# Optimization experiments

Measured on AMD Instinct MI355X. Metric: run time of the kernel, lower is better.

Reference implementation:

```python
import jax, jax.numpy as jnp
from jax import lax
import numpy as np

MS = 128            # local_map_size
HALF = MS // 2
B, S = 8, 64
C, H, W = 3, 1024, 1024


def setup_inputs() -> dict:
    key = jax.random.key(0)
    ks = jax.random.split(key, 48)
    r = lambda i, shape, s: jax.random.normal(ks[i], shape, jnp.float32) * s
    z = lambda *shape: jnp.zeros(shape, jnp.float32)
    o = lambda *shape: jnp.ones(shape, jnp.float32)
    return {
        "full_map": jax.random.normal(ks[0], (B, C, H, W), jnp.float32),
        "conditions": jax.random.uniform(ks[1], (B, 5), jnp.float32, 0.0, 1024.0),
        "input_seq": jax.random.uniform(ks[2], (B, S, 2), jnp.float32, 0.0, 1024.0),
        "steps_remaining": jax.random.uniform(ks[3], (B, S), jnp.float32, 0.0, 500.0),
        # LocalMapEncoder convs (OIHW) + batchnorm affine params
        "cw1": r(4, (16, 3, 3, 3), 0.2),   "cb1": z(16),  "g1": o(16),  "be1": z(16),
        "cw2": r(5, (32, 16, 3, 3), 0.1),  "cb2": z(32),  "g2": o(32),  "be2": z(32),
        "cw3": r(6, (64, 32, 3, 3), 0.07), "cb3": z(64),  "g3": o(64),  "be3": z(64),
        "cw4": r(7, (128, 64, 3, 3), 0.05),"cb4": z(128), "g4": o(128), "be4": z(128),
        "fw1": r(8, (512, 128 * 8 * 8), 0.01), "fb1": z(512),
        "fw2": r(9, (256, 512), 0.04),         "fb2": z(256),
        # ConditionEncoder (6 -> 128 -> 64)
        "ew1": r(10, (128, 6), 0.05),  "eb1": z(128),
        "ew2": r(11, (64, 128), 0.05), "eb2": z(64),
        # coord embedder (2 -> 32)
        "mw": r(12, (32, 2), 0.05), "mb": z(32),
        # 2-layer LSTM, torch gate order (i, f, g, o)
        "w_ih0": r(13, (4 * 256, 32), 0.05),  "w_hh0": r(14, (4 * 256, 256), 0.05),
        "b_ih0": z(4 * 256), "b_hh0": z(4 * 256),
        "w_ih1": r(15, (4 * 256, 256), 0.05), "w_hh1": r(16, (4 * 256, 256), 0.05),
        "b_ih1": z(4 * 256), "b_hh1": z(4 * 256),
        # context layer (256+256+64=576 -> 128 -> 64) and output (64 -> 2)
        "xw1": r(17, (128, 576), 0.04), "xb1": z(128),
        "xw2": r(18, (64, 128), 0.05),  "xb2": z(64),
        "ow": r(19, (2, 64), 0.1),      "ob": z(2),
    }


def _conv_bn_relu(x, w, b, g, be):
    # stride-2 3x3 conv, padding 1, NCHW/OIHW; BatchNorm in training mode (batch stats)
    y = lax.conv_general_dilated(x, w, (2, 2), ((1, 1), (1, 1)),
                                 dimension_numbers=("NCHW", "OIHW", "NCHW"))
    y = y + b[None, :, None, None]
    mu = y.mean((0, 2, 3), keepdims=True)
    var = y.var((0, 2, 3), keepdims=True)
    y = (y - mu) * lax.rsqrt(var + 1e-5) * g[None, :, None, None] + be[None, :, None, None]
    return jax.nn.relu(y)


def _lstm_layer(x, w_ih, w_hh, b_ih, b_hh):
    # x: [B, S, D] -> hidden states [B, S, Hd]
    bsz, hd = x.shape[0], w_hh.shape[1]
    bias = b_ih + b_hh
    def step(carry, xt):
        h, c = carry
        zg = xt @ w_ih.T + h @ w_hh.T + bias
        i, f, gg, oo = jnp.split(zg, 4, axis=-1)
        c = jax.nn.sigmoid(f) * c + jax.nn.sigmoid(i) * jnp.tanh(gg)
        h = jax.nn.sigmoid(oo) * jnp.tanh(c)
        return (h, c), h
    h0 = jnp.zeros((bsz, hd), x.dtype)
    _, hs = lax.scan(step, (h0, h0), x.transpose(1, 0, 2))
    return hs.transpose(1, 0, 2)


def reference(full_map, conditions, input_seq, steps_remaining,
              cw1, cb1, g1, be1, cw2, cb2, g2, be2,
              cw3, cb3, g3, be3, cw4, cb4, g4, be4,
              fw1, fb1, fw2, fb2, ew1, eb1, ew2, eb2, mw, mb,
              w_ih0, w_hh0, b_ih0, b_hh0, w_ih1, w_hh1, b_ih1, b_hh1,
              xw1, xb1, xw2, xb2, ow, ob):
    bsz, seq, _ = input_seq.shape
    # --- batched crop+pad gather (replaces host numpy loop): zero-pad map by
    # HALF on each side, then every crop is a dynamic_slice of size MS at (y, x).
    padded = jnp.pad(full_map, ((0, 0), (0, 0), (HALF, HALF), (HALF, HALF)))
    ys = input_seq[..., 0].astype(jnp.int32).reshape(-1)
    xs = input_seq[..., 1].astype(jnp.int32).reshape(-1)
    bidx = jnp.repeat(jnp.arange(bsz, dtype=jnp.int32), seq)
    crop_one = lambda b, y, x: lax.dynamic_slice(padded, (b, 0, y, x), (1, C, MS, MS))[0]
    crops = jax.vmap(crop_one)(bidx, ys, xs)              # [B*S, C, MS, MS]
    # --- LocalMapEncoder
    h = _conv_bn_relu(crops, cw1, cb1, g1, be1)
    h = _conv_bn_relu(h, cw2, cb2, g2, be2)
    h = _conv_bn_relu(h, cw3, cb3, g3, be3)
    h = _conv_bn_relu(h, cw4, cb4, g4, be4)               # [B*S, 128, 8, 8]
    h = h.reshape(h.shape[0], -1)
    h = jax.nn.relu(h @ fw1.T + fb1) @ fw2.T + fb2
    map_features = h.reshape(bsz, seq, -1)                # [B, S, 256]
    # --- ConditionEncoder on [conditions ++ steps_remaining]
    enh = jnp.concatenate(
        [jnp.broadcast_to(conditions[:, None, :], (bsz, seq, 5)),
         steps_remaining[..., None]], axis=-1)            # [B, S, 6]
    cond_features = jax.nn.relu(enh @ ew1.T + eb1) @ ew2.T + eb2  # [B, S, 64]
    # --- route predictor
    emb = jax.nn.relu(input_seq @ mw.T + mb)              # [B, S, 32]
    lstm_out = _lstm_layer(emb, w_ih0, w_hh0, b_ih0, b_hh0)
    lstm_out = _lstm_layer(lstm_out, w_ih1, w_hh1, b_ih1, b_hh1)  # [B, S, 256]
    combined = jnp.concatenate([lstm_out, map_features, cond_features], axis=-1)
    ctx = jax.nn.relu(jax.nn.relu(combined @ xw1.T + xb1) @ xw2.T + xb2)
    return ctx @ ow.T + ob                                # [B, S, 2]
```

## Files before the change

### kernel.cpp

```cpp
#include <hip/hip_runtime.h>

#define TPB 256
#define NLB 64

typedef float f32x4 __attribute__((ext_vector_type(4)));
typedef short bf16x8 __attribute__((ext_vector_type(8)));
typedef unsigned long long u64;

__device__ __forceinline__ float bf2f(unsigned short u) {
  union { unsigned int i; float f; } x; x.i = ((unsigned int)u) << 16; return x.f;
}
__device__ __forceinline__ unsigned short f2bf(float v) {
  union { float f; unsigned int i; } x; x.f = v;
  unsigned int r = (x.i + 0x7fffu + ((x.i >> 16) & 1u)) >> 16;
  return (unsigned short)r;
}
__device__ __forceinline__ float sigf(float x) { return 1.f / (1.f + __expf(-x)); }
__device__ __forceinline__ bf16x8 lda_bf8(const unsigned short* p) {
  union { uint4 u; bf16x8 v; } t; t.u = *(const uint4*)p; return t.v;
}
__device__ __forceinline__ bf16x8 frag_of(const unsigned int* w) {
  union { unsigned int u[4]; bf16x8 v; } t;
  t.u[0] = w[0]; t.u[1] = w[1]; t.u[2] = w[2]; t.u[3] = w[3]; return t.v;
}

__global__ __launch_bounds__(TPB, 2) void conv1_tap(
    const float* __restrict__ fmap, const float* __restrict__ iseq,
    const unsigned short* __restrict__ wT,
    const float* __restrict__ bias,
    unsigned short* __restrict__ out, float* __restrict__ part) {
  __shared__ __align__(16) unsigned short patch[17][132][8];
  __shared__ unsigned short Bsm[16][104];
  __shared__ float bs[16];
  __shared__ float swsum[4][16], swsq[4][16];
  const int tid = threadIdx.x;
  const int n = blockIdx.x >> 3, R0 = (blockIdx.x & 7) << 3;
  const int y = (int)iseq[n * 2], x = (int)iseq[n * 2 + 1];
  const int bimg = n >> 6;

  for (int e = tid; e < 1536; e += TPB) Bsm[e / 96][e % 96] = wT[e];
  if (tid < 16) bs[tid] = bias[tid];
  for (int e = tid; e < 17 * 132; e += TPB)
    *(uint4*)&patch[e / 132][e % 132][0] = uint4{0u, 0u, 0u, 0u};
  __syncthreads();
  for (int e = tid; e < 3 * 17 * 132; e += TPB) {
    int ic = e / 2244, rem = e % 2244, l = rem / 132, c = rem % 132;
    int i = 2 * R0 - 1 + l, j = c - 1;
    float v = 0.f;
    if ((unsigned)i < 128u && (unsigned)j < 128u) {
      int r = y + i - 64, cc = x + j - 64;
      if ((unsigned)r < 1024u && (unsigned)cc < 1024u)
        v = fmap[(((size_t)bimg * 3 + ic) << 20) + ((size_t)r << 10) + cc];
    }
    patch[l][c][ic] = f2bf(v);
  }
  __syncthreads();

  const int w = tid >> 6, lane = tid & 63, fr = lane & 15, kg = lane >> 4;
  f32x4 acc[8];
#pragma unroll
  for (int m = 0; m < 8; ++m) acc[m] = {0.f, 0.f, 0.f, 0.f};

#pragma unroll
  for (int ch = 0; ch < 3; ++ch) {
    int k8 = ch * 4 + kg;
    int ki = (k8 >= 9) ? 0 : ((k8 * 11) >> 5);
    int kj = (k8 >= 9) ? 0 : (k8 - 3 * ki);
    bf16x8 bfr = lda_bf8(&Bsm[fr][k8 * 8]);
#pragma unroll
    for (int m = 0; m < 8; ++m) {
      int p = w * 128 + m * 16 + fr;
      int pr = p >> 6, pc = p & 63;
      bf16x8 af = lda_bf8(&patch[2 * pr + ki][2 * pc + kj][0]);
      acc[m] = __builtin_amdgcn_mfma_f32_16x16x32_bf16(af, bfr, acc[m], 0, 0, 0);
    }
  }
  const int rg = lane >> 4;
  float bb = bs[fr];
  float sps = 0.f, spq = 0.f;
#pragma unroll
  for (int m = 0; m < 8; ++m) {
#pragma unroll
    for (int r = 0; r < 4; ++r) {
      int p = w * 128 + m * 16 + rg * 4 + r;
      int pr = p >> 6, pc = p & 63;
      float v = acc[m][r] + bb;
      sps += v; spq = fmaf(v, v, spq);
      out[(((size_t)n * 64 + R0 + pr) * 64 + pc) * 16 + fr] = f2bf(v);
    }
  }
  sps += __shfl_xor(sps, 16); spq += __shfl_xor(spq, 16);
  sps += __shfl_xor(sps, 32); spq += __shfl_xor(spq, 32);
  if (lane < 16) { swsum[w][fr] = sps; swsq[w][fr] = spq; }
  __syncthreads();
  if (tid < 16) {
    float s = swsum[0][tid] + swsum[1][tid] + swsum[2][tid] + swsum[3][tid];
    float q = swsq[0][tid] + swsq[1][tid] + swsq[2][tid] + swsq[3][tid];
    part[(size_t)blockIdx.x * 32 + tid * 2] = s;
    part[(size_t)blockIdx.x * 32 + tid * 2 + 1] = q;
  }
}

template<int CIN, int COUT_BLK, int NSPLIT, int HIN, int HOUT>
__global__ __launch_bounds__(TPB, 2) void conv_tap(
    const unsigned short* __restrict__ inb,
    const float* __restrict__ ss,
    const unsigned short* __restrict__ wT,
    const float* __restrict__ bias,
    unsigned short* __restrict__ out, float* __restrict__ part) {
  constexpr int K = CIN * 9;
  constexpr int K8 = K / 8;
  constexpr int NCH = (K8 + 3) / 4;
  constexpr int KPAD = NCH * 32;
  constexpr int BS = KPAD + 8;
  constexpr int CINP = CIN + 8;
  constexpr int ICG_SH = (CIN == 16) ? 1 : (CIN == 32) ? 2 : 3;
  constexpr int TPR = HOUT / 8;
  constexpr int TILES = TPR * TPR;
  constexpr int NT = COUT_BLK / 16;
  constexpr int COUT_TOT = COUT_BLK * NSPLIT;

  __shared__ unsigned short patch[289 * CINP];
  __shared__ unsigned short Bsm[COUT_BLK * BS];
  __shared__ float ssl[CIN * 2];
  __shared__ float swsum[4][COUT_BLK], swsq[4][COUT_BLK];

  const int tid = threadIdx.x;
  const int bid = blockIdx.x;
  const int n = bid / (TILES * NSPLIT);
  const int rem = bid % (TILES * NSPLIT);
  const int tile = rem / NSPLIT;
  const int split = rem % NSPLIT;
  const int TR0 = (tile / TPR) * 8, TC0 = (tile % TPR) * 8;
  const int oc0 = split * COUT_BLK;

  for (int i = tid; i < CIN * 2; i += TPB) ssl[i] = ss[i];
  __syncthreads();

  for (int e = tid; e < 289 * (CIN / 8); e += TPB) {
    int icg = e % (CIN / 8), pix = e / (CIN / 8);
    int row = pix / 17, col = pix % 17;
    int ir = 2 * TR0 - 1 + row, jc = 2 * TC0 - 1 + col;
    uint4 o = {0u, 0u, 0u, 0u};
    if ((unsigned)ir < (unsigned)HIN && (unsigned)jc < (unsigned)HIN) {
      uint4 v = *(const uint4*)&inb[(((size_t)n * HIN + ir) * HIN + jc) * CIN + icg * 8];
      unsigned int d[4] = {v.x, v.y, v.z, v.w};
      unsigned int* op = (unsigned int*)&o;
#pragma unroll
      for (int t = 0; t < 4; ++t) {
        int c = icg * 8 + 2 * t;
        float a = fmaxf(fmaf(bf2f((unsigned short)(d[t] & 0xffff)), ssl[2 * c], ssl[2 * c + 1]), 0.f);
        float b = fmaxf(fmaf(bf2f((unsigned short)(d[t] >> 16)), ssl[2 * c + 2], ssl[2 * c + 3]), 0.f);
        op[t] = (unsigned int)f2bf(a) | ((unsigned int)f2bf(b) << 16);
      }
    }
    *(uint4*)&patch[pix * CINP + icg * 8] = o;
  }
  constexpr int B8 = COUT_BLK * (KPAD / 8);
  for (int e = tid; e < B8; e += TPB) {
    int oc = e / (KPAD / 8), k8i = e % (KPAD / 8);
    uint4 v = {0u, 0u, 0u, 0u};
    if (k8i * 8 < K) v = *(const uint4*)&wT[(size_t)(oc0 + oc) * K + k8i * 8];
    *(uint4*)&Bsm[oc * BS + k8i * 8] = v;
  }
  __syncthreads();

  const int wave = tid >> 6, lane = tid & 63;
  const int fr = lane & 15, kg = lane >> 4;
  const int p = wave * 16 + fr;
  const int pr = p >> 3, pc = p & 7;
  f32x4 acc[NT];
#pragma unroll
  for (int j = 0; j < NT; ++j) acc[j] = {0.f, 0.f, 0.f, 0.f};

#pragma unroll
  for (int ch = 0; ch < NCH; ++ch) {
    int k8 = ch * 4 + kg;
    int tap = k8 >> ICG_SH, icg = k8 & ((1 << ICG_SH) - 1);
    int ki = (tap * 11) >> 5;
    int kj = tap - 3 * ki;
    int addr = ((2 * pr + ki) * 17 + (2 * pc + kj)) * CINP + icg * 8;
    if (tap >= 9) addr = 0;
    bf16x8 af = lda_bf8(&patch[addr]);
#pragma unroll
    for (int j = 0; j < NT; ++j) {
      bf16x8 bfr = lda_bf8(&Bsm[(j * 16 + fr) * BS + ch * 32 + kg * 8]);
      acc[j] = __builtin_amdgcn_mfma_f32_16x16x32_bf16(af, bfr, acc[j], 0, 0, 0);
    }
  }
  const int rg = lane >> 4;
#pragma unroll
  for (int j = 0; j < NT; ++j) {
    int oc = oc0 + j * 16 + fr;
    float bb = bias[oc];
    float s1 = 0.f, q1 = 0.f;
#pragma unroll
    for (int r = 0; r < 4; ++r) {
      int pp = wave * 16 + rg * 4 + r;
      int orow = TR0 + (pp >> 3), ocol = TC0 + (pp & 7);
      float v = acc[j][r] + bb;
      s1 += v; q1 = fmaf(v, v, q1);
      out[(((size_t)n * HOUT + orow) * HOUT + ocol) * COUT_TOT + oc] = f2bf(v);
    }
    s1 += __shfl_xor(s1, 16); q1 += __shfl_xor(q1, 16);
    s1 += __shfl_xor(s1, 32); q1 += __shfl_xor(q1, 32);
    if (lane < 16) { swsum[wave][j * 16 + fr] = s1; swsq[wave][j * 16 + fr] = q1; }
  }
  __syncthreads();
  if (tid < COUT_BLK) {
    float s = swsum[0][tid] + swsum[1][tid] + swsum[2][tid] + swsum[3][tid];
    float q = swsq[0][tid] + swsq[1][tid] + swsq[2][tid] + swsq[3][tid];
    part[(size_t)bid * COUT_BLK * 2 + tid * 2] = s;
    part[(size_t)bid * COUT_BLK * 2 + tid * 2 + 1] = q;
  }
}

__global__ __launch_bounds__(TPB) void stats_final3(const float* __restrict__ part,
    const float* __restrict__ gamma, const float* __restrict__ beta,
    float* __restrict__ ss, float inv_count, int COUT_BLK, int NSPLIT, int NBID) {
  const int c = blockIdx.x, tid = threadIdx.x;
  const int split = c / COUT_BLK, loc = c % COUT_BLK;
  const int NG = NBID / NSPLIT;
  float s = 0.f, q = 0.f;
  for (int g = tid; g < NG; g += TPB) {
    size_t b = (size_t)g * NSPLIT + split;
    s += part[b * COUT_BLK * 2 + loc * 2];
    q += part[b * COUT_BLK * 2 + loc * 2 + 1];
  }
  __shared__ float rs[TPB], rq[TPB];
  rs[tid] = s; rq[tid] = q;
  __syncthreads();
  for (int off = TPB / 2; off > 0; off >>= 1) {
    if (tid < off) { rs[tid] += rs[tid + off]; rq[tid] += rq[tid + off]; }
    __syncthreads();
  }
  if (tid == 0) {
    float mean = rs[0] * inv_count;
    float var  = rq[0] * inv_count - mean * mean;
    float rstd = rsqrtf(var + 1e-5f);
    float scl  = gamma[c] * rstd;
    ss[2 * c] = scl;
    ss[2 * c + 1] = beta[c] - mean * scl;
  }
}

__global__ __launch_bounds__(TPB) void prep_wt(
    const float* __restrict__ w1, const float* __restrict__ w2,
    const float* __restrict__ w3, const float* __restrict__ w4,
    unsigned short* __restrict__ wt1, unsigned short* __restrict__ wt2,
    unsigned short* __restrict__ wt3, unsigned short* __restrict__ wt4) {
  int i = blockIdx.x * TPB + threadIdx.x;
  if (i < 1536) {
    int oc = i / 96, k = i % 96;
    int tap = k >> 3, ic = k & 7;
    float v = (tap < 9 && ic < 3) ? w1[(oc * 3 + ic) * 9 + tap] : 0.f;
    wt1[i] = f2bf(v);
  } else if (i < 6144) {
    int j = i - 1536;
    int oc = j / 144, k = j % 144;
    wt2[j] = f2bf(w2[(oc * 16 + (k & 15)) * 9 + (k >> 4)]);
  } else if (i < 24576) {
    int j = i - 6144;
    int oc = j / 288, k = j % 288;
    wt3[j] = f2bf(w3[(oc * 32 + (k & 31)) * 9 + (k >> 5)]);
  } else if (i < 98304) {
    int j = i - 24576;
    int oc = j / 576, k = j % 576;
    wt4[j] = f2bf(w4[(oc * 64 + (k & 63)) * 9 + (k >> 6)]);
  }
}

__global__ __launch_bounds__(TPB) void permute_fw1(const float* __restrict__ in,
    unsigned short* __restrict__ out) {
  __shared__ unsigned short l[128 * 66];
  int n = blockIdx.x;
  for (int e = threadIdx.x; e < 8192; e += TPB) {
    int c = e >> 6, pix = e & 63;
    l[c * 66 + pix] = f2bf(in[(size_t)n * 8192 + e]);
  }
  __syncthreads();
  for (int e = threadIdx.x; e < 8192; e += TPB) {
    int pix = e >> 7, c = e & 127;
    out[(size_t)n * 8192 + e] = l[c * 66 + pix];
  }
}

__device__ __forceinline__ uint4 bnpack(uint4 v, const float* sst) {
  unsigned int d[4] = {v.x, v.y, v.z, v.w};
  uint4 o; unsigned int* op = (unsigned int*)&o;
#pragma unroll
  for (int t = 0; t < 4; ++t) {
    float a = fmaxf(fmaf(bf2f((unsigned short)(d[t] & 0xffff)), sst[4 * t], sst[4 * t + 1]), 0.f);
    float b = fmaxf(fmaf(bf2f((unsigned short)(d[t] >> 16)), sst[4 * t + 2], sst[4 * t + 3]), 0.f);
    op[t] = (unsigned int)f2bf(a) | ((unsigned int)f2bf(b) << 16);
  }
  return o;
}

__global__ __launch_bounds__(TPB, 2) void fc1_mfma(
    const unsigned short* __restrict__ A, const unsigned short* __restrict__ W,
    const float* __restrict__ ss, const float* __restrict__ bias,
    float* __restrict__ out) {
  __shared__ unsigned short As[64][64];
  __shared__ unsigned short Bs[64][64];
  __shared__ float ssl[256];
  const int tid = threadIdx.x;
  const int lane = tid & 63, wave = tid >> 6;
  const int wr = (wave >> 1) * 32, wc = (wave & 1) * 32;
  const int bm = blockIdx.y * 64, bn = blockIdx.x * 64;
  f32x4 acc00 = {0.f, 0.f, 0.f, 0.f}, acc01 = acc00, acc10 = acc00, acc11 = acc00;
  const int r0 = tid >> 3, c0 = tid & 7;
  const int fr = lane & 15, kg = lane >> 4;
  for (int i = tid; i < 256; i += TPB) ssl[i] = ss[i];
  __syncthreads();
  for (int kt = 0; kt < 128; ++kt) {
    const int kb = kt * 64;
    uint4 av0 = *(const uint4*)&A[(size_t)(bm + r0) * 8192 + kb + c0 * 8];
    uint4 av1 = *(const uint4*)&A[(size_t)(bm + r0 + 32) * 8192 + kb + c0 * 8];
    uint4 bv0 = *(const uint4*)&W[(size_t)(bn + r0) * 8192 + kb + c0 * 8];
    uint4 bv1 = *(const uint4*)&W[(size_t)(bn + r0 + 32) * 8192 + kb + c0 * 8];
    const float* sst = &ssl[2 * ((kb + c0 * 8) & 127)];
    __syncthreads();
    av0 = bnpack(av0, sst);
    av1 = bnpack(av1, sst);
    *(uint4*)&As[r0][(c0 ^ (r0 & 7)) * 8] = av0;
    *(uint4*)&As[r0 + 32][(c0 ^ (r0 & 7)) * 8] = av1;
    *(uint4*)&Bs[r0][(c0 ^ (r0 & 7)) * 8] = bv0;
    *(uint4*)&Bs[r0 + 32][(c0 ^ (r0 & 7)) * 8] = bv1;
    __syncthreads();
#pragma unroll
    for (int ks = 0; ks < 2; ++ks) {
      int ch = ks * 4 + kg;
      int ra0 = wr + fr, ra1 = wr + 16 + fr;
      int rb0 = wc + fr, rb1 = wc + 16 + fr;
      bf16x8 a_0 = lda_bf8(&As[ra0][(ch ^ (ra0 & 7)) * 8]);
      bf16x8 a_1 = lda_bf8(&As[ra1][(ch ^ (ra1 & 7)) * 8]);
      bf16x8 b_0 = lda_bf8(&Bs[rb0][(ch ^ (rb0 & 7)) * 8]);
      bf16x8 b_1 = lda_bf8(&Bs[rb1][(ch ^ (rb1 & 7)) * 8]);
      acc00 = __builtin_amdgcn_mfma_f32_16x16x32_bf16(a_0, b_0, acc00, 0, 0, 0);
      acc01 = __builtin_amdgcn_mfma_f32_16x16x32_bf16(a_0, b_1, acc01, 0, 0, 0);
      acc10 = __builtin_amdgcn_mfma_f32_16x16x32_bf16(a_1, b_0, acc10, 0, 0, 0);
      acc11 = __builtin_amdgcn_mfma_f32_16x16x32_bf16(a_1, b_1, acc11, 0, 0, 0);
    }
  }
  const int rg = lane >> 4;
  int n0 = bn + wc + fr, n1 = n0 + 16;
  float bi0 = bias[n0], bi1 = bias[n1];
#pragma unroll
  for (int r = 0; r < 4; ++r) {
    int m0 = bm + wr + rg * 4 + r, m1 = m0 + 16;
    out[m0 * 512 + n0] = fmaxf(acc00[r] + bi0, 0.f);
    out[m0 * 512 + n1] = fmaxf(acc01[r] + bi1, 0.f);
    out[m1 * 512 + n0] = fmaxf(acc10[r] + bi0, 0.f);
    out[m1 * 512 + n1] = fmaxf(acc11[r] + bi1, 0.f);
  }
}

__global__ __launch_bounds__(TPB, 2) void gemm_m64(
    const float* __restrict__ A, const float* __restrict__ W,
    const float* __restrict__ bias, float* __restrict__ out,
    int N, int K, int relu, int ldo, int coff) {
  __shared__ unsigned short As[64 * 40];
  __shared__ unsigned short Bs[64 * 40];
  const int tid = threadIdx.x, lane = tid & 63, wave = tid >> 6;
  const int wr = (wave >> 1) * 32, wc = (wave & 1) * 32;
  const int bm = blockIdx.y * 64, bn = blockIdx.x * 64;
  const int fr = lane & 15, kg = lane >> 4;
  const int sr = tid >> 2, sc = (tid & 3) * 8;
  f32x4 a00 = {0.f, 0.f, 0.f, 0.f}, a01 = a00, a10 = a00, a11 = a00;
  int nch = (K + 31) >> 5;
  for (int ch = 0; ch < nch; ++ch) {
    int kb = ch * 32;
    __syncthreads();
    {
      unsigned short tmp[8];
#pragma unroll
      for (int j = 0; j < 8; ++j) {
        int k = kb + sc + j;
        tmp[j] = (k < K) ? f2bf(A[(size_t)(bm + sr) * K + k]) : (unsigned short)0;
      }
      *(uint4*)&As[sr * 40 + sc] = *(const uint4*)tmp;
      int wrow = bn + sr;
#pragma unroll
      for (int j = 0; j < 8; ++j) {
        int k = kb + sc + j;
        tmp[j] = (wrow < N && k < K) ? f2bf(W[(size_t)wrow * K + k]) : (unsigned short)0;
      }
      *(uint4*)&Bs[sr * 40 + sc] = *(const uint4*)tmp;
    }
    __syncthreads();
    bf16x8 af0 = lda_bf8(&As[(wr + fr) * 40 + kg * 8]);
    bf16x8 af1 = lda_bf8(&As[(wr + 16 + fr) * 40 + kg * 8]);
    bf16x8 bf0 = lda_bf8(&Bs[(wc + fr) * 40 + kg * 8]);
    bf16x8 bf1 = lda_bf8(&Bs[(wc + 16 + fr) * 40 + kg * 8]);
    a00 = __builtin_amdgcn_mfma_f32_16x16x32_bf16(af0, bf0, a00, 0, 0, 0);
    a01 = __builtin_amdgcn_mfma_f32_16x16x32_bf16(af0, bf1, a01, 0, 0, 0);
    a10 = __builtin_amdgcn_mfma_f32_16x16x32_bf16(af1, bf0, a10, 0, 0, 0);
    a11 = __builtin_amdgcn_mfma_f32_16x16x32_bf16(af1, bf1, a11, 0, 0, 0);
  }
  const int rg = lane >> 4;
  int n0 = bn + wc + fr, n1 = n0 + 16;
  float bi0 = (n0 < N) ? bias[n0] : 0.f;
  float bi1 = (n1 < N) ? bias[n1] : 0.f;
#pragma unroll
  for (int r = 0; r < 4; ++r) {
    int m0 = bm + wr + rg * 4 + r, m1 = m0 + 16;
    if (n0 < N) {
      float v = a00[r] + bi0; out[(size_t)m0 * ldo + coff + n0] = relu ? fmaxf(v, 0.f) : v;
      v = a10[r] + bi0;       out[(size_t)m1 * ldo + coff + n0] = relu ? fmaxf(v, 0.f) : v;
    }
    if (n1 < N) {
      float v = a01[r] + bi1; out[(size_t)m0 * ldo + coff + n1] = relu ? fmaxf(v, 0.f) : v;
      v = a11[r] + bi1;       out[(size_t)m1 * ldo + coff + n1] = relu ? fmaxf(v, 0.f) : v;
    }
  }
}

__global__ __launch_bounds__(TPB) void cond_enc(
    const float* __restrict__ cond, const float* __restrict__ steps,
    const float* __restrict__ ew1, const float* __restrict__ eb1,
    const float* __restrict__ ew2, const float* __restrict__ eb2,
    float* __restrict__ comb) {
  __shared__ float w1s[128][8];
  __shared__ float w2s[64][132];
  __shared__ float hbuf[64][132];
  const int tid = threadIdx.x;
  const int row0 = blockIdx.x * 64;
  for (int e = tid; e < 128 * 8; e += TPB) {
    int k = e >> 3, t = e & 7;
    w1s[k][t] = (t < 6) ? ew1[k * 6 + t] : (t == 6 ? eb1[k] : 0.f);
  }
  for (int e = tid; e < 64 * 128; e += TPB) {
    int j = e >> 7, k = e & 127;
    w2s[j][k] = ew2[j * 128 + k];
  }
  __syncthreads();
  {
    int row = tid >> 2, ks = tid & 3;
    int n = row0 + row;
    int b = n >> 6, s = n & 63;
    float e0 = cond[b * 5], e1 = cond[b * 5 + 1], e2 = cond[b * 5 + 2];
    float e3 = cond[b * 5 + 3], e4 = cond[b * 5 + 4];
    float e5 = steps[b * 64 + s];
    for (int k = ks * 32; k < ks * 32 + 32; ++k) {
      float a = fmaf(w1s[k][0], e0, fmaf(w1s[k][1], e1, fmaf(w1s[k][2], e2,
                fmaf(w1s[k][3], e3, fmaf(w1s[k][4], e4, fmaf(w1s[k][5], e5, w1s[k][6]))))));
      hbuf[row][k] = fmaxf(a, 0.f);
    }
  }
  __syncthreads();
  {
    int row = tid >> 2, js = tid & 3;
    int n = row0 + row;
    for (int j = js * 16; j < js * 16 + 16; ++j) {
      float a = eb2[j];
#pragma unroll 8
      for (int k = 0; k < 128; ++k) a = fmaf(w2s[j][k], hbuf[row][k], a);
      comb[(size_t)n * 576 + 512 + j] = a;
    }
  }
}

__global__ __launch_bounds__(TPB, 1) void lstm_kernel(
    const float* __restrict__ iseq,
    const float* __restrict__ mw, const float* __restrict__ mb,
    const float* __restrict__ w_ih0, const float* __restrict__ w_hh0,
    const float* __restrict__ b_ih0, const float* __restrict__ b_hh0,
    const float* __restrict__ w_ih1, const float* __restrict__ w_hh1,
    const float* __restrict__ b_ih1, const float* __restrict__ b_hh1,
    u64* __restrict__ h0x, u64* __restrict__ h1x,
    float* __restrict__ comb) {
  const int tid = threadIdx.x;
  const int blkid = blockIdx.x;
  const int u0 = blkid * 4;

  __shared__ float xz[64][8][16];
  __shared__ __align__(16) char reg2[18944];
  __shared__ float bias1s[16];

  float (*embc)[8][32] = (float (*)[8][32])reg2;
  float* mwmb = (float*)(reg2 + 16384);
  unsigned short (*v0s)[264] = (unsigned short (*)[264])reg2;
  unsigned short (*w1h)[264] = (unsigned short (*)[264])(reg2 + 8448);
  float (*P0)[16]  = (float (*)[16])(reg2 + 16896);
  float (*P1a)[16] = (float (*)[16])(reg2 + 17408);
  float (*P1b)[16] = (float (*)[16])(reg2 + 17920);

  const int wv = tid >> 6, lane = tid & 63, fr = lane & 15, kg = lane >> 4;
  const int r = tid & 15, ks = tid >> 4;
  const int R  = (r >> 2) * 256 + u0 + (r & 3);
  const int Rf = (fr >> 2) * 256 + u0 + (fr & 3);

  unsigned int wfrag[8][4];
  {
    const float* wsrc = (wv == 0) ? w_hh0 : (wv == 1) ? w_ih1 : w_hh1;
#pragma unroll
    for (int ch = 0; ch < 8; ++ch)
#pragma unroll
      for (int d = 0; d < 4; ++d) {
        float lo = wsrc[(size_t)Rf * 256 + ch * 32 + kg * 8 + d * 2];
        float hi = wsrc[(size_t)Rf * 256 + ch * 32 + kg * 8 + d * 2 + 1];
        wfrag[ch][d] = (unsigned)f2bf(lo) | ((unsigned)f2bf(hi) << 16);
      }
  }
  float wtmp[32];
#pragma unroll
  for (int i = 0; i < 32; ++i) wtmp[i] = w_ih0[R * 32 + i];
  const float bias0r = b_ih0[R] + b_hh0[R];
  if (tid < 16) bias1s[tid] = b_ih1[R] + b_hh1[R];
  if (tid < 96) mwmb[tid] = (tid < 64) ? mw[tid] : mb[tid - 64];
  __syncthreads();

  for (int chunk = 0; chunk < 4; ++chunk) {
    if (tid < 128) {
      int pp = tid >> 3, b = tid & 7;
      int pg = chunk * 16 + pp;
      float s0 = iseq[(b * 64 + pg) * 2 + 0];
      float s1 = iseq[(b * 64 + pg) * 2 + 1];
      for (int k = 0; k < 32; ++k)
        embc[pp][b][k] = fmaxf(fmaf(mwmb[2 * k], s0, fmaf(mwmb[2 * k + 1], s1, mwmb[64 + k])), 0.f);
    }
    __syncthreads();
    {
      int pg = chunk * 16 + ks;
      for (int b = 0; b < 8; ++b) {
        float a = bias0r;
        const float* e = &embc[ks][b][0];
#pragma unroll
        for (int k = 0; k < 32; ++k) a = fmaf(wtmp[k], e[k], a);
        xz[pg][b][r] = a;
      }
    }
    __syncthreads();
  }

  for (int i = tid; i < 8 * 264; i += TPB) {
    v0s[8 + i / 264][i % 264] = 0;
    w1h[8 + i / 264][i % 264] = 0;
  }
  __syncthreads();

  float c0 = 0.f, c1 = 0.f;
  for (int p = 0; p <= 64; ++p) {
    if (tid < 128) {
      if (p >= 1) {
        const unsigned tag0 = (unsigned)p;
        const u64* s0p = &h0x[(size_t)(p - 1) * 1024 + tid * 8];
        u64 e[8];
        for (;;) {
          bool ok = true;
#pragma unroll
          for (int i = 0; i < 8; ++i) {
            e[i] = __hip_atomic_load(&s0p[i], __ATOMIC_RELAXED, __HIP_MEMORY_SCOPE_AGENT);
            ok &= ((unsigned)(e[i] >> 32) == tag0);
          }
          if (ok) break;
          __builtin_amdgcn_s_sleep(1);
        }
#pragma unroll
        for (int i = 0; i < 8; ++i) {
          int g = tid * 8 + i;
          int bb = (g >> 1) & 7, ub = (g >> 4) * 4 + (g & 1) * 2;
          *(unsigned int*)&v0s[bb][ub] = (unsigned int)e[i];
        }
      } else {
#pragma unroll
        for (int i = 0; i < 8; ++i) {
          int g = tid * 8 + i;
          int bb = (g >> 1) & 7, ub = (g >> 4) * 4 + (g & 1) * 2;
          *(unsigned int*)&v0s[bb][ub] = 0u;
        }
      }
    } else {
      int t2 = tid - 128;
      if (p >= 2) {
        const unsigned tag1 = (unsigned)(p - 1);
        const u64* s1p = &h1x[(size_t)(p - 2) * 1024 + t2 * 8];
        u64 e[8];
        for (;;) {
          bool ok = true;
#pragma unroll
          for (int i = 0; i < 8; ++i) {
            e[i] = __hip_atomic_load(&s1p[i], __ATOMIC_RELAXED, __HIP_MEMORY_SCOPE_AGENT);
            ok &= ((unsigned)(e[i] >> 32) == tag1);
          }
          if (ok) break;
          __builtin_amdgcn_s_sleep(1);
        }
#pragma unroll
        for (int i = 0; i < 8; ++i) {
          int g = t2 * 8 + i;
          int bb = (g >> 1) & 7, ub = (g >> 4) * 4 + (g & 1) * 2;
          *(unsigned int*)&w1h[bb][ub] = (unsigned int)e[i];
        }
      } else {
#pragma unroll
        for (int i = 0; i < 8; ++i) {
          int g = t2 * 8 + i;
          int bb = (g >> 1) & 7, ub = (g >> 4) * 4 + (g & 1) * 2;
          *(unsigned int*)&w1h[bb][ub] = 0u;
        }
      }
    }
    __syncthreads();

    if (wv == 0) {
      if (p < 64) {
        f32x4 acc = {0.f, 0.f, 0.f, 0.f};
#pragma unroll
        for (int ch = 0; ch < 8; ++ch) {
          bf16x8 af = lda_bf8(&v0s[fr][ch * 32 + kg * 8]);
          acc = __builtin_amdgcn_mfma_f32_16x16x32_bf16(af, frag_of(wfrag[ch]), acc, 0, 0, 0);
        }
#pragma unroll
        for (int j = 0; j < 4; ++j) {
          int bb2 = (lane >> 4) * 4 + j;
          if (bb2 < 8) P0[bb2][fr] = acc[j];
        }
      }
    } else if (wv == 1) {
      if (p >= 1) {
        f32x4 acc = {0.f, 0.f, 0.f, 0.f};
#pragma unroll
        for (int ch = 0; ch < 8; ++ch) {
          bf16x8 af = lda_bf8(&v0s[fr][ch * 32 + kg * 8]);
          acc = __builtin_amdgcn_mfma_f32_16x16x32_bf16(af, frag_of(wfrag[ch]), acc, 0, 0, 0);
        }
#pragma unroll
        for (int j = 0; j < 4; ++j) {
          int bb2 = (lane >> 4) * 4 + j;
          if (bb2 < 8) P1a[bb2][fr] = acc[j];
        }
      }
    } else if (wv == 2) {
      if (p >= 1) {
        f32x4 acc = {0.f, 0.f, 0.f, 0.f};
#pragma unroll
        for (int ch = 0; ch < 8; ++ch) {
          bf16x8 af = lda_bf8(&w1h[fr][ch * 32 + kg * 8]);
          acc = __builtin_amdgcn_mfma_f32_16x16x32_bf16(af, frag_of(wfrag[ch]), acc, 0, 0, 0);
        }
#pragma unroll
        for (int j = 0; j < 4; ++j) {
          int bb2 = (lane >> 4) * 4 + j;
          if (bb2 < 8) P1b[bb2][fr] = acc[j];
        }
      }
    }
    __syncthreads();

    if (tid < 32 && p < 64) {
      int b = tid >> 2, uu = tid & 3;
      float zi = P0[b][uu]      + xz[p][b][uu];
      float zf = P0[b][4 + uu]  + xz[p][b][4 + uu];
      float zg = P0[b][8 + uu]  + xz[p][b][8 + uu];
      float zo = P0[b][12 + uu] + xz[p][b][12 + uu];
      c0 = sigf(zf) * c0 + sigf(zi) * tanhf(zg);
      float h = sigf(zo) * tanhf(c0);
      float hp = __shfl_xor(h, 1);
      if (!(uu & 1)) {
        unsigned int d = (unsigned int)f2bf(h) | ((unsigned int)f2bf(hp) << 16);
        u64 v = ((u64)(unsigned)(p + 1) << 32) | d;
        __hip_atomic_store(&h0x[(size_t)p * 1024 + blkid * 16 + b * 2 + (uu >> 1)], v,
                           __ATOMIC_RELAXED, __HIP_MEMORY_SCOPE_AGENT);
      }
    } else if (tid >= 32 && tid < 64 && p >= 1) {
      int t2 = tid - 32, b = t2 >> 2, uu = t2 & 3;
      float zi = P1a[b][uu]      + P1b[b][uu]      + bias1s[uu];
      float zf = P1a[b][4 + uu]  + P1b[b][4 + uu]  + bias1s[4 + uu];
      float zg = P1a[b][8 + uu]  + P1b[b][8 + uu]  + bias1s[8 + uu];
      float zo = P1a[b][12 + uu] + P1b[b][12 + uu] + bias1s[12 + uu];
      c1 = sigf(zf) * c1 + sigf(zi) * tanhf(zg);
      float h = sigf(zo) * tanhf(c1);
      comb[(size_t)(b * 64 + (p - 1)) * 576 + u0 + uu] = h;
      float hp = __shfl_xor(h, 1);
      if (!(uu & 1)) {
        unsigned int d = (unsigned int)f2bf(h) | ((unsigned int)f2bf(hp) << 16);
        u64 v = ((u64)(unsigned)p << 32) | d;
        __hip_atomic_store(&h1x[(size_t)(p - 1) * 1024 + blkid * 16 + b * 2 + (uu >> 1)], v,
                           __ATOMIC_RELAXED, __HIP_MEMORY_SCOPE_AGENT);
      }
    }
  }
}

extern "C" void kernel_launch(void* const* d_in, const int* in_sizes, int n_in,
                              void* d_out, int out_size, void* d_ws, size_t ws_size,
                              hipStream_t stream) {
  const float* fmap  = (const float*)d_in[0];
  const float* cond  = (const float*)d_in[1];
  const float* iseq  = (const float*)d_in[2];
  const float* steps = (const float*)d_in[3];
  const float* cw1 = (const float*)d_in[4];  const float* cb1 = (const float*)d_in[5];
  const float* g1  = (const float*)d_in[6];  const float* be1 = (const float*)d_in[7];
  const float* cw2 = (const float*)d_in[8];  const float* cb2 = (const float*)d_in[9];
  const float* g2  = (const float*)d_in[10]; const float* be2 = (const float*)d_in[11];
  const float* cw3 = (const float*)d_in[12]; const float* cb3 = (const float*)d_in[13];
  const float* g3  = (const float*)d_in[14]; const float* be3 = (const float*)d_in[15];
  const float* cw4 = (const float*)d_in[16]; const float* cb4 = (const float*)d_in[17];
  const float* g4  = (const float*)d_in[18]; const float* be4 = (const float*)d_in[19];
  const float* fw1 = (const float*)d_in[20]; const float* fb1 = (const float*)d_in[21];
  const float* fw2 = (const float*)d_in[22]; const float* fb2 = (const float*)d_in[23];
  const float* ew1 = (const float*)d_in[24]; const float* eb1 = (const float*)d_in[25];
  const float* ew2 = (const float*)d_in[26]; const float* eb2 = (const float*)d_in[27];
  const float* mw  = (const float*)d_in[28]; const float* mb  = (const float*)d_in[29];
  const float* w_ih0 = (const float*)d_in[30]; const float* w_hh0 = (const float*)d_in[31];
  const float* b_ih0 = (const float*)d_in[32]; const float* b_hh0 = (const float*)d_in[33];
  const float* w_ih1 = (const float*)d_in[34]; const float* w_hh1 = (const float*)d_in[35];
  const float* b_ih1 = (const float*)d_in[36]; const float* b_hh1 = (const float*)d_in[37];
  const float* xw1 = (const float*)d_in[38]; const float* xb1 = (const float*)d_in[39];
  const float* xw2 = (const float*)d_in[40]; const float* xb2 = (const float*)d_in[41];
  const float* ow  = (const float*)d_in[42]; const float* ob  = (const float*)d_in[43];

  float* ws = (float*)d_ws;
  unsigned short* y1bf  = (unsigned short*)ws;
  unsigned short* y2bf  = (unsigned short*)(ws + 16777216);
  unsigned short* y3bf  = (unsigned short*)(ws + 25165824);
  unsigned short* y4pre = (unsigned short*)(ws + 29360128);
  unsigned short* fw1bf = (unsigned short*)(ws + 33554432);
  size_t base = 35651584;
  float* part  = ws + base; base += 524288;
  float* ss1   = ws + base; base += 32;
  float* ss2   = ws + base; base += 64;
  float* ss3   = ws + base; base += 128;
  float* ss4   = ws + base; base += 256;
  float* f1    = ws + base; base += 262144;
  u64*   h0x   = (u64*)(ws + base); base += 131072;
  u64*   h1x   = (u64*)(ws + base); base += 131072;
  float* comb  = ws + base; base += 294912;
  float* cx1   = ws + base; base += 65536;
  float* cx2   = ws + base; base += 32768;
  unsigned short* wt1 = (unsigned short*)(ws + base); base += 768;
  unsigned short* wt2 = (unsigned short*)(ws + base); base += 2304;
  unsigned short* wt3 = (unsigned short*)(ws + base); base += 9216;
  unsigned short* wt4 = (unsigned short*)(ws + base); base += 36864;

  prep_wt<<<384, TPB, 0, stream>>>(cw1, cw2, cw3, cw4, wt1, wt2, wt3, wt4);
  permute_fw1<<<512, TPB, 0, stream>>>(fw1, fw1bf);

  conv1_tap<<<4096, TPB, 0, stream>>>(fmap, iseq, wt1, cb1, y1bf, part);
  stats_final3<<<16, TPB, 0, stream>>>(part, g1, be1, ss1, 1.f / 2097152.f, 16, 1, 4096);
  conv_tap<16, 32, 1, 64, 32><<<8192, TPB, 0, stream>>>(y1bf, ss1, wt2, cb2, y2bf, part);
  stats_final3<<<32, TPB, 0, stream>>>(part, g2, be2, ss2, 1.f / 524288.f, 32, 1, 8192);
  conv_tap<32, 64, 1, 32, 16><<<2048, TPB, 0, stream>>>(y2bf, ss2, wt3, cb3, y3bf, part);
  stats_final3<<<64, TPB, 0, stream>>>(part, g3, be3, ss3, 1.f / 131072.f, 64, 1, 2048);
  conv_tap<64, 32, 4, 16, 8><<<2048, TPB, 0, stream>>>(y3bf, ss3, wt4, cb4, y4pre, part);
  stats_final3<<<128, TPB, 0, stream>>>(part, g4, be4, ss4, 1.f / 32768.f, 32, 4, 2048);

  hipMemsetAsync(h0x, 0, 2 * 64 * 1024 * sizeof(u64), stream);
  lstm_kernel<<<NLB, TPB, 0, stream>>>(iseq, mw, mb,
                                       w_ih0, w_hh0, b_ih0, b_hh0,
                                       w_ih1, w_hh1, b_ih1, b_hh1,
                                       h0x, h1x, comb);

  fc1_mfma<<<dim3(8, 8), TPB, 0, stream>>>(y4pre, fw1bf, ss4, fb1, f1);
  gemm_m64<<<dim3(4, 8), TPB, 0, stream>>>(f1, fw2, fb2, comb, 256, 512, 0, 576, 256);

  cond_enc<<<8, TPB, 0, stream>>>(cond, steps, ew1, eb1, ew2, eb2, comb);

  gemm_m64<<<dim3(2, 8), TPB, 0, stream>>>(comb, xw1, xb1, cx1, 128, 576, 1, 128, 0);
  gemm_m64<<<dim3(1, 8), TPB, 0, stream>>>(cx1, xw2, xb2, cx2, 64, 128, 1, 64, 0);
  gemm_m64<<<dim3(1, 8), TPB, 0, stream>>>(cx2, ow, ob, (float*)d_out, 2, 64, 0, 2, 0);
}
```

Before: 675.5 us.

## Fuse conv, BN-stats, LSTM and MLP stages into one persistent megakernel

Replaces the chain of separate conv, BatchNorm-statistics, LSTM, fc and gemm launches with a single persistent kernel of 448 blocks. 384 blocks loop over the conv tiles and meet at atomic grid barriers between stages. The remaining 64 blocks appear to run the LSTM concurrently, and the final gemms wait on a flag it sets. Conv weights are kept resident in shared memory across tiles, and per-block BN partials are accumulated before being written. The aim is to remove launch gaps and overlap the LSTM with the conv stack. The cost is fewer blocks per conv stage, spin-wait barriers that depend on all blocks being co-resident, and a deadlock risk if they are not.

```diff
diff --git a/kernel.cpp b/kernel.cpp
--- a/kernel.cpp
+++ b/kernel.cpp
@@ -2,6 +2,8 @@
 
 #define TPB 256
 #define NLB 64
+#define NCW 384
+#define NBLK 448
 
 typedef float f32x4 __attribute__((ext_vector_type(4)));
 typedef short bf16x8 __attribute__((ext_vector_type(8)));
@@ -23,91 +25,59 @@
   union { unsigned int u[4]; bf16x8 v; } t;
   t.u[0] = w[0]; t.u[1] = w[1]; t.u[2] = w[2]; t.u[3] = w[3]; return t.v;
 }
-
-__global__ __launch_bounds__(TPB, 2) void conv1_tap(
-    const float* __restrict__ fmap, const float* __restrict__ iseq,
-    const unsigned short* __restrict__ wT,
-    const float* __restrict__ bias,
-    unsigned short* __restrict__ out, float* __restrict__ part) {
-  __shared__ __align__(16) unsigned short patch[17][132][8];
-  __shared__ unsigned short Bsm[16][104];
-  __shared__ float bs[16];
-  __shared__ float swsum[4][16], swsq[4][16];
+__device__ __forceinline__ uint4 bnpack(uint4 v, const float* sst) {
+  unsigned int d[4] = {v.x, v.y, v.z, v.w};
+  uint4 o; unsigned int* op = (unsigned int*)&o;
+#pragma unroll
+  for (int t = 0; t < 4; ++t) {
+    float a = fmaxf(fmaf(bf2f((unsigned short)(d[t] & 0xffff)), sst[4 * t], sst[4 * t + 1]), 0.f);
+    float b = fmaxf(fmaf(bf2f((unsigned short)(d[t] >> 16)), sst[4 * t + 2], sst[4 * t + 3]), 0.f);
+    op[t] = (unsigned int)f2bf(a) | ((unsigned int)f2bf(b) << 16);
+  }
+  return o;
+}
+
+__device__ __forceinline__ void cbar(int* bar, int idx) {
+  __syncthreads();
+  if (threadIdx.x == 0) {
+    __hip_atomic_fetch_add(&bar[idx], 1, __ATOMIC_RELEASE, __HIP_MEMORY_SCOPE_AGENT);
+    while (__hip_atomic_load(&bar[idx], __ATOMIC_RELAXED, __HIP_MEMORY_SCOPE_AGENT) < NCW)
+      __builtin_amdgcn_s_sleep(8);
+    (void)__hip_atomic_load(&bar[idx], __ATOMIC_ACQUIRE, __HIP_MEMORY_SCOPE_AGENT);
+  }
+  __syncthreads();
+}
+
+__device__ void ssr(const float* part, const float* gamma, const float* beta,
+                    float* ss, float inv_count, int c, float* red) {
   const int tid = threadIdx.x;
-  const int n = blockIdx.x >> 3, R0 = (blockIdx.x & 7) << 3;
-  const int y = (int)iseq[n * 2], x = (int)iseq[n * 2 + 1];
-  const int bimg = n >> 6;
-
-  for (int e = tid; e < 1536; e += TPB) Bsm[e / 96][e % 96] = wT[e];
-  if (tid < 16) bs[tid] = bias[tid];
-  for (int e = tid; e < 17 * 132; e += TPB)
-    *(uint4*)&patch[e / 132][e % 132][0] = uint4{0u, 0u, 0u, 0u};
-  __syncthreads();
-  for (int e = tid; e < 3 * 17 * 132; e += TPB) {
-    int ic = e / 2244, rem = e % 2244, l = rem / 132, c = rem % 132;
-    int i = 2 * R0 - 1 + l, j = c - 1;
-    float v = 0.f;
-    if ((unsigned)i < 128u && (unsigned)j < 128u) {
-      int r = y + i - 64, cc = x + j - 64;
-      if ((unsigned)r < 1024u && (unsigned)cc < 1024u)
-        v = fmap[(((size_t)bimg * 3 + ic) << 20) + ((size_t)r << 10) + cc];
-    }
-    patch[l][c][ic] = f2bf(v);
-  }
-  __syncthreads();
-
-  const int w = tid >> 6, lane = tid & 63, fr = lane & 15, kg = lane >> 4;
-  f32x4 acc[8];
-#pragma unroll
-  for (int m = 0; m < 8; ++m) acc[m] = {0.f, 0.f, 0.f, 0.f};
-
-#pragma unroll
-  for (int ch = 0; ch < 3; ++ch) {
-    int k8 = ch * 4 + kg;
-    int ki = (k8 >= 9) ? 0 : ((k8 * 11) >> 5);
-    int kj = (k8 >= 9) ? 0 : (k8 - 3 * ki);
-    bf16x8 bfr = lda_bf8(&Bsm[fr][k8 * 8]);
-#pragma unroll
-    for (int m = 0; m < 8; ++m) {
-      int p = w * 128 + m * 16 + fr;
-      int pr = p >> 6, pc = p & 63;
-      bf16x8 af = lda_bf8(&patch[2 * pr + ki][2 * pc + kj][0]);
-      acc[m] = __builtin_amdgcn_mfma_f32_16x16x32_bf16(af, bfr, acc[m], 0, 0, 0);
-    }
-  }
-  const int rg = lane >> 4;
-  float bb = bs[fr];
-  float sps = 0.f, spq = 0.f;
-#pragma unroll
-  for (int m = 0; m < 8; ++m) {
-#pragma unroll
-    for (int r = 0; r < 4; ++r) {
-      int p = w * 128 + m * 16 + rg * 4 + r;
-      int pr = p >> 6, pc = p & 63;
-      float v = acc[m][r] + bb;
-      sps += v; spq = fmaf(v, v, spq);
-      out[(((size_t)n * 64 + R0 + pr) * 64 + pc) * 16 + fr] = f2bf(v);
-    }
-  }
-  sps += __shfl_xor(sps, 16); spq += __shfl_xor(spq, 16);
-  sps += __shfl_xor(sps, 32); spq += __shfl_xor(spq, 32);
-  if (lane < 16) { swsum[w][fr] = sps; swsq[w][fr] = spq; }
-  __syncthreads();
-  if (tid < 16) {
-    float s = swsum[0][tid] + swsum[1][tid] + swsum[2][tid] + swsum[3][tid];
-    float q = swsq[0][tid] + swsq[1][tid] + swsq[2][tid] + swsq[3][tid];
-    part[(size_t)blockIdx.x * 32 + tid * 2] = s;
-    part[(size_t)blockIdx.x * 32 + tid * 2 + 1] = q;
-  }
-}
-
-template<int CIN, int COUT_BLK, int NSPLIT, int HIN, int HOUT>
-__global__ __launch_bounds__(TPB, 2) void conv_tap(
-    const unsigned short* __restrict__ inb,
-    const float* __restrict__ ss,
-    const unsigned short* __restrict__ wT,
-    const float* __restrict__ bias,
-    unsigned short* __restrict__ out, float* __restrict__ part) {
+  float s = 0.f, q = 0.f;
+  for (int g = tid; g < NCW; g += TPB) {
+    s += part[(size_t)g * 256 + c * 2];
+    q += part[(size_t)g * 256 + c * 2 + 1];
+  }
+  red[tid] = s; red[256 + tid] = q;
+  __syncthreads();
+  for (int off = TPB / 2; off > 0; off >>= 1) {
+    if (tid < off) { red[tid] += red[tid + off]; red[256 + tid] += red[256 + tid + off]; }
+    __syncthreads();
+  }
+  if (tid == 0) {
+    float mean = red[0] * inv_count;
+    float var  = red[256] * inv_count - mean * mean;
+    float rstd = rsqrtf(var + 1e-5f);
+    float scl  = gamma[c] * rstd;
+    ss[2 * c] = scl;
+    ss[2 * c + 1] = beta[c] - mean * scl;
+  }
+}
+
+template<int CIN, int CB, int NS, int HIN, int HOUT>
+__device__ void ctap_tile(
+    const unsigned short* __restrict__ inb, const unsigned short* __restrict__ wT,
+    const float* __restrict__ bias, unsigned short* __restrict__ out,
+    int t, unsigned short* patch, unsigned short* Bsm, const float* ssl,
+    float* swsum, float* swsq, float* racc_s, float* racc_q) {
   constexpr int K = CIN * 9;
   constexpr int K8 = K / 8;
   constexpr int NCH = (K8 + 3) / 4;
@@ -117,26 +87,18 @@
   constexpr int ICG_SH = (CIN == 16) ? 1 : (CIN == 32) ? 2 : 3;
   constexpr int TPR = HOUT / 8;
   constexpr int TILES = TPR * TPR;
-  constexpr int NT = COUT_BLK / 16;
-  constexpr int COUT_TOT = COUT_BLK * NSPLIT;
-
-  __shared__ unsigned short patch[289 * CINP];
-  __shared__ unsigned short Bsm[COUT_BLK * BS];
-  __shared__ float ssl[CIN * 2];
-  __shared__ float swsum[4][COUT_BLK], swsq[4][COUT_BLK];
+  constexpr int NT = CB / 16;
+  constexpr int COUT_TOT = CB * NS;
 
   const int tid = threadIdx.x;
-  const int bid = blockIdx.x;
-  const int n = bid / (TILES * NSPLIT);
-  const int rem = bid % (TILES * NSPLIT);
-  const int tile = rem / NSPLIT;
-  const int split = rem % NSPLIT;
+  const int n = t / (TILES * NS);
+  const int rem = t % (TILES * NS);
+  const int tile = rem / NS;
+  const int split = rem % NS;
   const int TR0 = (tile / TPR) * 8, TC0 = (tile % TPR) * 8;
-  const int oc0 = split * COUT_BLK;
-
-  for (int i = tid; i < CIN * 2; i += TPB) ssl[i] = ss[i];
-  __syncthreads();
-
+  const int oc0 = split * CB;
+
+  __syncthreads();
   for (int e = tid; e < 289 * (CIN / 8); e += TPB) {
     int icg = e % (CIN / 8), pix = e / (CIN / 8);
     int row = pix / 17, col = pix % 17;
@@ -147,21 +109,22 @@
       unsigned int d[4] = {v.x, v.y, v.z, v.w};
       unsigned int* op = (unsigned int*)&o;
 #pragma unroll
-      for (int t = 0; t < 4; ++t) {
-        int c = icg * 8 + 2 * t;
-        float a = fmaxf(fmaf(bf2f((unsigned short)(d[t] & 0xffff)), ssl[2 * c], ssl[2 * c + 1]), 0.f);
-        float b = fmaxf(fmaf(bf2f((unsigned short)(d[t] >> 16)), ssl[2 * c + 2], ssl[2 * c + 3]), 0.f);
-        op[t] = (unsigned int)f2bf(a) | ((unsigned int)f2bf(b) << 16);
+      for (int tt = 0; tt < 4; ++tt) {
+        int c = icg * 8 + 2 * tt;
+        float a = fmaxf(fmaf(bf2f((unsigned short)(d[tt] & 0xffff)), ssl[2 * c], ssl[2 * c + 1]), 0.f);
+        float b = fmaxf(fmaf(bf2f((unsigned short)(d[tt] >> 16)), ssl[2 * c + 2], ssl[2 * c + 3]), 0.f);
+        op[tt] = (unsigned int)f2bf(a) | ((unsigned int)f2bf(b) << 16);
       }
     }
     *(uint4*)&patch[pix * CINP + icg * 8] = o;
   }
-  constexpr int B8 = COUT_BLK * (KPAD / 8);
-  for (int e = tid; e < B8; e += TPB) {
-    int oc = e / (KPAD / 8), k8i = e % (KPAD / 8);
-    uint4 v = {0u, 0u, 0u, 0u};
-    if (k8i * 8 < K) v = *(const uint4*)&wT[(size_t)(oc0 + oc) * K + k8i * 8];
-    *(uint4*)&Bsm[oc * BS + k8i * 8] = v;
+  if (NS > 1) {
+    for (int e = tid; e < CB * (KPAD / 8); e += TPB) {
+      int oc = e / (KPAD / 8), k8i = e % (KPAD / 8);
+      uint4 v = {0u, 0u, 0u, 0u};
+      if (k8i * 8 < K) v = *(const uint4*)&wT[(size_t)(oc0 + oc) * K + k8i * 8];
+      *(uint4*)&Bsm[oc * BS + k8i * 8] = v;
+    }
   }
   __syncthreads();
 
@@ -204,43 +167,130 @@
     }
     s1 += __shfl_xor(s1, 16); q1 += __shfl_xor(q1, 16);
     s1 += __shfl_xor(s1, 32); q1 += __shfl_xor(q1, 32);
-    if (lane < 16) { swsum[wave][j * 16 + fr] = s1; swsq[wave][j * 16 + fr] = q1; }
-  }
-  __syncthreads();
-  if (tid < COUT_BLK) {
-    float s = swsum[0][tid] + swsum[1][tid] + swsum[2][tid] + swsum[3][tid];
-    float q = swsq[0][tid] + swsq[1][tid] + swsq[2][tid] + swsq[3][tid];
-    part[(size_t)bid * COUT_BLK * 2 + tid * 2] = s;
-    part[(size_t)bid * COUT_BLK * 2 + tid * 2 + 1] = q;
-  }
-}
-
-__global__ __launch_bounds__(TPB) void stats_final3(const float* __restrict__ part,
-    const float* __restrict__ gamma, const float* __restrict__ beta,
-    float* __restrict__ ss, float inv_count, int COUT_BLK, int NSPLIT, int NBID) {
-  const int c = blockIdx.x, tid = threadIdx.x;
-  const int split = c / COUT_BLK, loc = c % COUT_BLK;
-  const int NG = NBID / NSPLIT;
-  float s = 0.f, q = 0.f;
-  for (int g = tid; g < NG; g += TPB) {
-    size_t b = (size_t)g * NSPLIT + split;
-    s += part[b * COUT_BLK * 2 + loc * 2];
-    q += part[b * COUT_BLK * 2 + loc * 2 + 1];
-  }
-  __shared__ float rs[TPB], rq[TPB];
-  rs[tid] = s; rq[tid] = q;
-  __syncthreads();
-  for (int off = TPB / 2; off > 0; off >>= 1) {
-    if (tid < off) { rs[tid] += rs[tid + off]; rq[tid] += rq[tid + off]; }
-    __syncthreads();
-  }
-  if (tid == 0) {
-    float mean = rs[0] * inv_count;
-    float var  = rq[0] * inv_count - mean * mean;
-    float rstd = rsqrtf(var + 1e-5f);
-    float scl  = gamma[c] * rstd;
-    ss[2 * c] = scl;
-    ss[2 * c + 1] = beta[c] - mean * scl;
+    if (lane < 16) { swsum[wave * CB + j * 16 + fr] = s1; swsq[wave * CB + j * 16 + fr] = q1; }
+  }
+  __syncthreads();
+  if (tid < CB) {
+    float s = swsum[tid] + swsum[CB + tid] + swsum[2 * CB + tid] + swsum[3 * CB + tid];
+    float q = swsq[tid] + swsq[CB + tid] + swsq[2 * CB + tid] + swsq[3 * CB + tid];
+    racc_s[oc0 + tid] += s; racc_q[oc0 + tid] += q;
+  }
+}
+
+__device__ void dev_gemm64(const float* __restrict__ A, const float* __restrict__ W,
+    const float* __restrict__ bias, float* __restrict__ out,
+    int N, int K, int relu, int ldo, int coff, int bm, int bn, char* sm) {
+  unsigned short* As = (unsigned short*)sm;
+  unsigned short* Bs = (unsigned short*)(sm + 5120);
+  const int tid = threadIdx.x, lane = tid & 63, wave = tid >> 6;
+  const int wr = (wave >> 1) * 32, wc = (wave & 1) * 32;
+  const int fr = lane & 15, kg = lane >> 4;
+  const int sr = tid >> 2, sc = (tid & 3) * 8;
+  f32x4 a00 = {0.f, 0.f, 0.f, 0.f}, a01 = a00, a10 = a00, a11 = a00;
+  int nch = (K + 31) >> 5;
+  for (int ch = 0; ch < nch; ++ch) {
+    int kb = ch * 32;
+    __syncthreads();
+    {
+      unsigned short tmp[8];
+#pragma unroll
+      for (int j = 0; j < 8; ++j) {
+        int k = kb + sc + j;
+        tmp[j] = (k < K) ? f2bf(A[(size_t)(bm + sr) * K + k]) : (unsigned short)0;
+      }
+      *(uint4*)&As[sr * 40 + sc] = *(const uint4*)tmp;
+      int wrow = bn + sr;
+#pragma unroll
+      for (int j = 0; j < 8; ++j) {
+        int k = kb + sc + j;
+        tmp[j] = (wrow < N && k < K) ? f2bf(W[(size_t)wrow * K + k]) : (unsigned short)0;
+      }
+      *(uint4*)&Bs[sr * 40 + sc] = *(const uint4*)tmp;
+    }
+    __syncthreads();
+    bf16x8 af0 = lda_bf8(&As[(wr + fr) * 40 + kg * 8]);
+    bf16x8 af1 = lda_bf8(&As[(wr + 16 + fr) * 40 + kg * 8]);
+    bf16x8 bf0 = lda_bf8(&Bs[(wc + fr) * 40 + kg * 8]);
+    bf16x8 bf1 = lda_bf8(&Bs[(wc + 16 + fr) * 40 + kg * 8]);
+    a00 = __builtin_amdgcn_mfma_f32_16x16x32_bf16(af0, bf0, a00, 0, 0, 0);
+    a01 = __builtin_amdgcn_mfma_f32_16x16x32_bf16(af0, bf1, a01, 0, 0, 0);
+    a10 = __builtin_amdgcn_mfma_f32_16x16x32_bf16(af1, bf0, a10, 0, 0, 0);
+    a11 = __builtin_amdgcn_mfma_f32_16x16x32_bf16(af1, bf1, a11, 0, 0, 0);
+  }
+  __syncthreads();
+  const int rg = lane >> 4;
+  int n0 = bn + wc + fr, n1 = n0 + 16;
+  float bi0 = (n0 < N) ? bias[n0] : 0.f;
+  float bi1 = (n1 < N) ? bias[n1] : 0.f;
+#pragma unroll
+  for (int r = 0; r < 4; ++r) {
+    int m0 = bm + wr + rg * 4 + r, m1 = m0 + 16;
+    if (n0 < N) {
+      float v = a00[r] + bi0; out[(size_t)m0 * ldo + coff + n0] = relu ? fmaxf(v, 0.f) : v;
+      v = a10[r] + bi0;       out[(size_t)m1 * ldo + coff + n0] = relu ? fmaxf(v, 0.f) : v;
+    }
+    if (n1 < N) {
+      float v = a01[r] + bi1; out[(size_t)m0 * ldo + coff + n1] = relu ? fmaxf(v, 0.f) : v;
+      v = a11[r] + bi1;       out[(size_t)m1 * ldo + coff + n1] = relu ? fmaxf(v, 0.f) : v;
+    }
+  }
+}
+
+__device__ void dev_fc1(const unsigned short* __restrict__ A, const unsigned short* __restrict__ W,
+    const float* __restrict__ ss, const float* __restrict__ bias, float* __restrict__ out,
+    int bm, int bn, char* sm) {
+  unsigned short (*As)[64] = (unsigned short (*)[64])sm;
+  unsigned short (*Bs)[64] = (unsigned short (*)[64])(sm + 8192);
+  float* ssl = (float*)(sm + 16384);
+  const int tid = threadIdx.x;
+  const int lane = tid & 63, wave = tid >> 6;
+  const int wr = (wave >> 1) * 32, wc = (wave & 1) * 32;
+  f32x4 acc00 = {0.f, 0.f, 0.f, 0.f}, acc01 = acc00, acc10 = acc00, acc11 = acc00;
+  const int r0 = tid >> 3, c0 = tid & 7;
+  const int fr = lane & 15, kg = lane >> 4;
+  for (int i = tid; i < 256; i += TPB) ssl[i] = ss[i];
+  __syncthreads();
+  for (int kt = 0; kt < 128; ++kt) {
+    const int kb = kt * 64;
+    uint4 av0 = *(const uint4*)&A[(size_t)(bm + r0) * 8192 + kb + c0 * 8];
+    uint4 av1 = *(const uint4*)&A[(size_t)(bm + r0 + 32) * 8192 + kb + c0 * 8];
+    uint4 bv0 = *(const uint4*)&W[(size_t)(bn + r0) * 8192 + kb + c0 * 8];
+    uint4 bv1 = *(const uint4*)&W[(size_t)(bn + r0 + 32) * 8192 + kb + c0 * 8];
+    const float* sst = &ssl[2 * ((kb + c0 * 8) & 127)];
+    __syncthreads();
+    av0 = bnpack(av0, sst);
+    av1 = bnpack(av1, sst);
+    *(uint4*)&As[r0][(c0 ^ (r0 & 7)) * 8] = av0;
+    *(uint4*)&As[r0 + 32][(c0 ^ (r0 & 7)) * 8] = av1;
+    *(uint4*)&Bs[r0][(c0 ^ (r0 & 7)) * 8] = bv0;
+    *(uint4*)&Bs[r0 + 32][(c0 ^ (r0 & 7)) * 8] = bv1;
+    __syncthreads();
+#pragma unroll
+    for (int ks = 0; ks < 2; ++ks) {
+      int ch = ks * 4 + kg;
+      int ra0 = wr + fr, ra1 = wr + 16 + fr;
+      int rb0 = wc + fr, rb1 = wc + 16 + fr;
+      bf16x8 a_0 = lda_bf8(&As[ra0][(ch ^ (ra0 & 7)) * 8]);
+      bf16x8 a_1 = lda_bf8(&As[ra1][(ch ^ (ra1 & 7)) * 8]);
+      bf16x8 b_0 = lda_bf8(&Bs[rb0][(ch ^ (rb0 & 7)) * 8]);
+      bf16x8 b_1 = lda_bf8(&Bs[rb1][(ch ^ (rb1 & 7)) * 8]);
+      acc00 = __builtin_amdgcn_mfma_f32_16x16x32_bf16(a_0, b_0, acc00, 0, 0, 0);
+      acc01 = __builtin_amdgcn_mfma_f32_16x16x32_bf16(a_0, b_1, acc01, 0, 0, 0);
+      acc10 = __builtin_amdgcn_mfma_f32_16x16x32_bf16(a_1, b_0, acc10, 0, 0, 0);
+      acc11 = __builtin_amdgcn_mfma_f32_16x16x32_bf16(a_1, b_1, acc11, 0, 0, 0);
+    }
+  }
+  __syncthreads();
+  const int rg = lane >> 4;
+  int n0 = bn + wc + fr, n1 = n0 + 16;
+  float bi0 = bias[n0], bi1 = bias[n1];
+#pragma unroll
+  for (int r = 0; r < 4; ++r) {
+    int m0 = bm + wr + rg * 4 + r, m1 = m0 + 16;
+    out[m0 * 512 + n0] = fmaxf(acc00[r] + bi0, 0.f);
+    out[m0 * 512 + n1] = fmaxf(acc01[r] + bi1, 0.f);
+    out[m1 * 512 + n0] = fmaxf(acc10[r] + bi0, 0.f);
+    out[m1 * 512 + n1] = fmaxf(acc11[r] + bi1, 0.f);
   }
 }
 
@@ -285,403 +335,452 @@
   }
 }
 
-__device__ __forceinline__ uint4 bnpack(uint4 v, const float* sst) {
-  unsigned int d[4] = {v.x, v.y, v.z, v.w};
-  uint4 o; unsigned int* op = (unsigned int*)&o;
-#pragma unroll
-  for (int t = 0; t < 4; ++t) {
-    float a = fmaxf(fmaf(bf2f((unsigned short)(d[t] & 0xffff)), sst[4 * t], sst[4 * t + 1]), 0.f);
-    float b = fmaxf(fmaf(bf2f((unsigned short)(d[t] >> 16)), sst[4 * t + 2], sst[4 * t + 3]), 0.f);
-    op[t] = (unsigned int)f2bf(a) | ((unsigned int)f2bf(b) << 16);
-  }
-  return o;
-}
-
-__global__ __launch_bounds__(TPB, 2) void fc1_mfma(
-    const unsigned short* __restrict__ A, const unsigned short* __restrict__ W,
-    const float* __restrict__ ss, const float* __restrict__ bias,
-    float* __restrict__ out) {
-  __shared__ unsigned short As[64][64];
-  __shared__ unsigned short Bs[64][64];
-  __shared__ float ssl[256];
-  const int tid = threadIdx.x;
-  const int lane = tid & 63, wave = tid >> 6;
-  const int wr = (wave >> 1) * 32, wc = (wave & 1) * 32;
-  const int bm = blockIdx.y * 64, bn = blockIdx.x * 64;
-  f32x4 acc00 = {0.f, 0.f, 0.f, 0.f}, acc01 = acc00, acc10 = acc00, acc11 = acc00;
-  const int r0 = tid >> 3, c0 = tid & 7;
-  const int fr = lane & 15, kg = lane >> 4;
-  for (int i = tid; i < 256; i += TPB) ssl[i] = ss[i];
-  __syncthreads();
-  for (int kt = 0; kt < 128; ++kt) {
-    const int kb = kt * 64;
-    uint4 av0 = *(const uint4*)&A[(size_t)(bm + r0) * 8192 + kb + c0 * 8];
-    uint4 av1 = *(const uint4*)&A[(size_t)(bm + r0 + 32) * 8192 + kb + c0 * 8];
-    uint4 bv0 = *(const uint4*)&W[(size_t)(bn + r0) * 8192 + kb + c0 * 8];
-    uint4 bv1 = *(const uint4*)&W[(size_t)(bn + r0 + 32) * 8192 + kb + c0 * 8];
-    const float* sst = &ssl[2 * ((kb + c0 * 8) & 127)];
-    __syncthreads();
-    av0 = bnpack(av0, sst);
-    av1 = bnpack(av1, sst);
-    *(uint4*)&As[r0][(c0 ^ (r0 & 7)) * 8] = av0;
-    *(uint4*)&As[r0 + 32][(c0 ^ (r0 & 7)) * 8] = av1;
-    *(uint4*)&Bs[r0][(c0 ^ (r0 & 7)) * 8] = bv0;
-    *(uint4*)&Bs[r0 + 32][(c0 ^ (r0 & 7)) * 8] = bv1;
-    __syncthreads();
-#pragma unroll
-    for (int ks = 0; ks < 2; ++ks) {
-      int ch = ks * 4 + kg;
-      int ra0 = wr + fr, ra1 = wr + 16 + fr;
-      int rb0 = wc + fr, rb1 = wc + 16 + fr;
-      bf16x8 a_0 = lda_bf8(&As[ra0][(ch ^ (ra0 & 7)) * 8]);
-      bf16x8 a_1 = lda_bf8(&As[ra1][(ch ^ (ra1 & 7)) * 8]);
-      bf16x8 b_0 = lda_bf8(&Bs[rb0][(ch ^ (rb0 & 7)) * 8]);
-      bf16x8 b_1 = lda_bf8(&Bs[rb1][(ch ^ (rb1 & 7)) * 8]);
-      acc00 = __builtin_amdgcn_mfma_f32_16x16x32_bf16(a_0, b_0, acc00, 0, 0, 0);
-      acc01 = __builtin_amdgcn_mfma_f32_16x16x32_bf16(a_0, b_1, acc01, 0, 0, 0);
-      acc10 = __builtin_amdgcn_mfma_f32_16x16x32_bf16(a_1, b_0, acc10, 0, 0, 0);
-      acc11 = __builtin_amdgcn_mfma_f32_16x16x32_bf16(a_1, b_1, acc11, 0, 0, 0);
-    }
-  }
-  const int rg = lane >> 4;
-  int n0 = bn + wc + fr, n1 = n0 + 16;
-  float bi0 = bias[n0], bi1 = bias[n1];
-#pragma unroll
-  for (int r = 0; r < 4; ++r) {
-    int m0 = bm + wr + rg * 4 + r, m1 = m0 + 16;
-    out[m0 * 512 + n0] = fmaxf(acc00[r] + bi0, 0.f);
-    out[m0 * 512 + n1] = fmaxf(acc01[r] + bi1, 0.f);
-    out[m1 * 512 + n0] = fmaxf(acc10[r] + bi0, 0.f);
-    out[m1 * 512 + n1] = fmaxf(acc11[r] + bi1, 0.f);
-  }
-}
-
-__global__ __launch_bounds__(TPB, 2) void gemm_m64(
-    const float* __restrict__ A, const float* __restrict__ W,
-    const float* __restrict__ bias, float* __restrict__ out,
-    int N, int K, int relu, int ldo, int coff) {
-  __shared__ unsigned short As[64 * 40];
-  __shared__ unsigned short Bs[64 * 40];
-  const int tid = threadIdx.x, lane = tid & 63, wave = tid >> 6;
-  const int wr = (wave >> 1) * 32, wc = (wave & 1) * 32;
-  const int bm = blockIdx.y * 64, bn = blockIdx.x * 64;
-  const int fr = lane & 15, kg = lane >> 4;
-  const int sr = tid >> 2, sc = (tid & 3) * 8;
-  f32x4 a00 = {0.f, 0.f, 0.f, 0.f}, a01 = a00, a10 = a00, a11 = a00;
-  int nch = (K + 31) >> 5;
-  for (int ch = 0; ch < nch; ++ch) {
-    int kb = ch * 32;
-    __syncthreads();
-    {
-      unsigned short tmp[8];
-#pragma unroll
-      for (int j = 0; j < 8; ++j) {
-        int k = kb + sc + j;
-        tmp[j] = (k < K) ? f2bf(A[(size_t)(bm + sr) * K + k]) : (unsigned short)0;
-      }
-      *(uint4*)&As[sr * 40 + sc] = *(const uint4*)tmp;
-      int wrow = bn + sr;
-#pragma unroll
-      for (int j = 0; j < 8; ++j) {
-        int k = kb + sc + j;
-        tmp[j] = (wrow < N && k < K) ? f2bf(W[(size_t)wrow * K + k]) : (unsigned short)0;
-      }
-      *(uint4*)&Bs[sr * 40 + sc] = *(const uint4*)tmp;
-    }
-    __syncthreads();
-    bf16x8 af0 = lda_bf8(&As[(wr + fr) * 40 + kg * 8]);
-    bf16x8 af1 = lda_bf8(&As[(wr + 16 + fr) * 40 + kg * 8]);
-    bf16x8 bf0 = lda_bf8(&Bs[(wc + fr) * 40 + kg * 8]);
-    bf16x8 bf1 = lda_bf8(&Bs[(wc + 16 + fr) * 40 + kg * 8]);
-    a00 = __builtin_amdgcn_mfma_f32_16x16x32_bf16(af0, bf0, a00, 0, 0, 0);
-    a01 = __builtin_amdgcn_mfma_f32_16x16x32_bf16(af0, bf1, a01, 0, 0, 0);
-    a10 = __builtin_amdgcn_mfma_f32_16x16x32_bf16(af1, bf0, a10, 0, 0, 0);
-    a11 = __builtin_amdgcn_mfma_f32_16x16x32_bf16(af1, bf1, a11, 0, 0, 0);
-  }
-  const int rg = lane >> 4;
-  int n0 = bn + wc + fr, n1 = n0 + 16;
-  float bi0 = (n0 < N) ? bias[n0] : 0.f;
-  float bi1 = (n1 < N) ? bias[n1] : 0.f;
-#pragma unroll
-  for (int r = 0; r < 4; ++r) {
-    int m0 = bm + wr + rg * 4 + r, m1 = m0 + 16;
-    if (n0 < N) {
-      float v = a00[r] + bi0; out[(size_t)m0 * ldo + coff + n0] = relu ? fmaxf(v, 0.f) : v;
-      v = a10[r] + bi0;       out[(size_t)m1 * ldo + coff + n0] = relu ? fmaxf(v, 0.f) : v;
-    }
-    if (n1 < N) {
-      float v = a01[r] + bi1; out[(size_t)m0 * ldo + coff + n1] = relu ? fmaxf(v, 0.f) : v;
-      v = a11[r] + bi1;       out[(size_t)m1 * ldo + coff + n1] = relu ? fmaxf(v, 0.f) : v;
-    }
-  }
-}
-
-__global__ __launch_bounds__(TPB) void cond_enc(
-    const float* __restrict__ cond, const float* __restrict__ steps,
+__global__ __launch_bounds__(TPB, 2) void mega_kernel(
+    const float* __restrict__ fmap, const float* __restrict__ cond,
+    const float* __restrict__ iseq, const float* __restrict__ steps,
+    const unsigned short* __restrict__ wt1, const unsigned short* __restrict__ wt2,
+    const unsigned short* __restrict__ wt3, const unsigned short* __restrict__ wt4,
+    const float* __restrict__ cb1, const float* __restrict__ cb2,
+    const float* __restrict__ cb3, const float* __restrict__ cb4,
+    const float* __restrict__ g1, const float* __restrict__ be1,
+    const float* __restrict__ g2, const float* __restrict__ be2,
+    const float* __restrict__ g3, const float* __restrict__ be3,
+    const float* __restrict__ g4, const float* __restrict__ be4,
+    const unsigned short* __restrict__ fw1bf, const float* __restrict__ fb1,
+    const float* __restrict__ fw2, const float* __restrict__ fb2,
     const float* __restrict__ ew1, const float* __restrict__ eb1,
     const float* __restrict__ ew2, const float* __restrict__ eb2,
-    float* __restrict__ comb) {
-  __shared__ float w1s[128][8];
-  __shared__ float w2s[64][132];
-  __shared__ float hbuf[64][132];
-  const int tid = threadIdx.x;
-  const int row0 = blockIdx.x * 64;
-  for (int e = tid; e < 128 * 8; e += TPB) {
-    int k = e >> 3, t = e & 7;
-    w1s[k][t] = (t < 6) ? ew1[k * 6 + t] : (t == 6 ? eb1[k] : 0.f);
-  }
-  for (int e = tid; e < 64 * 128; e += TPB) {
-    int j = e >> 7, k = e & 127;
-    w2s[j][k] = ew2[j * 128 + k];
-  }
-  __syncthreads();
-  {
-    int row = tid >> 2, ks = tid & 3;
-    int n = row0 + row;
-    int b = n >> 6, s = n & 63;
-    float e0 = cond[b * 5], e1 = cond[b * 5 + 1], e2 = cond[b * 5 + 2];
-    float e3 = cond[b * 5 + 3], e4 = cond[b * 5 + 4];
-    float e5 = steps[b * 64 + s];
-    for (int k = ks * 32; k < ks * 32 + 32; ++k) {
-      float a = fmaf(w1s[k][0], e0, fmaf(w1s[k][1], e1, fmaf(w1s[k][2], e2,
-                fmaf(w1s[k][3], e3, fmaf(w1s[k][4], e4, fmaf(w1s[k][5], e5, w1s[k][6]))))));
-      hbuf[row][k] = fmaxf(a, 0.f);
-    }
-  }
-  __syncthreads();
-  {
-    int row = tid >> 2, js = tid & 3;
-    int n = row0 + row;
-    for (int j = js * 16; j < js * 16 + 16; ++j) {
-      float a = eb2[j];
-#pragma unroll 8
-      for (int k = 0; k < 128; ++k) a = fmaf(w2s[j][k], hbuf[row][k], a);
-      comb[(size_t)n * 576 + 512 + j] = a;
-    }
-  }
-}
-
-__global__ __launch_bounds__(TPB, 1) void lstm_kernel(
-    const float* __restrict__ iseq,
     const float* __restrict__ mw, const float* __restrict__ mb,
     const float* __restrict__ w_ih0, const float* __restrict__ w_hh0,
     const float* __restrict__ b_ih0, const float* __restrict__ b_hh0,
     const float* __restrict__ w_ih1, const float* __restrict__ w_hh1,
     const float* __restrict__ b_ih1, const float* __restrict__ b_hh1,
-    u64* __restrict__ h0x, u64* __restrict__ h1x,
-    float* __restrict__ comb) {
+    const float* __restrict__ xw1, const float* __restrict__ xb1,
+    const float* __restrict__ xw2, const float* __restrict__ xb2,
+    const float* __restrict__ oww, const float* __restrict__ obb,
+    unsigned short* __restrict__ y1bf, unsigned short* __restrict__ y2bf,
+    unsigned short* __restrict__ y3bf, unsigned short* __restrict__ y4pre,
+    float* __restrict__ part, float* ss1, float* ss2, float* ss3, float* ss4,
+    float* __restrict__ f1, u64* __restrict__ h0x, u64* __restrict__ h1x,
+    float* __restrict__ comb, float* __restrict__ cx1, float* __restrict__ cx2,
+    float* __restrict__ d_out, int* __restrict__ bar) {
+  __shared__ __align__(16) char sm[63488];
+  __shared__ float racc_s[128], racc_q[128];
   const int tid = threadIdx.x;
-  const int blkid = blockIdx.x;
-  const int u0 = blkid * 4;
-
-  __shared__ float xz[64][8][16];
-  __shared__ __align__(16) char reg2[18944];
-  __shared__ float bias1s[16];
-
-  float (*embc)[8][32] = (float (*)[8][32])reg2;
-  float* mwmb = (float*)(reg2 + 16384);
-  unsigned short (*v0s)[264] = (unsigned short (*)[264])reg2;
-  unsigned short (*w1h)[264] = (unsigned short (*)[264])(reg2 + 8448);
-  float (*P0)[16]  = (float (*)[16])(reg2 + 16896);
-  float (*P1a)[16] = (float (*)[16])(reg2 + 17408);
-  float (*P1b)[16] = (float (*)[16])(reg2 + 17920);
-
-  const int wv = tid >> 6, lane = tid & 63, fr = lane & 15, kg = lane >> 4;
-  const int r = tid & 15, ks = tid >> 4;
-  const int R  = (r >> 2) * 256 + u0 + (r & 3);
-  const int Rf = (fr >> 2) * 256 + u0 + (fr & 3);
-
-  unsigned int wfrag[8][4];
+
+  if (blockIdx.x < NLB) {
+    const int blkid = blockIdx.x;
+    const int u0 = blkid * 4;
+    float (*xz)[8][16] = (float (*)[8][16])sm;
+    char* reg2 = sm + 32768;
+    float* bias1s = (float*)(sm + 32768 + 18944);
+
+    float (*embc)[8][32] = (float (*)[8][32])reg2;
+    float* mwmb = (float*)(reg2 + 16384);
+    unsigned short (*v0s)[264] = (unsigned short (*)[264])reg2;
+    unsigned short (*w1h)[264] = (unsigned short (*)[264])(reg2 + 8448);
+    float (*P0)[16]  = (float (*)[16])(reg2 + 16896);
+    float (*P1a)[16] = (float (*)[16])(reg2 + 17408);
+    float (*P1b)[16] = (float (*)[16])(reg2 + 17920);
+
+    const int wv = tid >> 6, lane = tid & 63, fr = lane & 15, kg = lane >> 4;
+    const int r = tid & 15, ks = tid >> 4;
+    const int R  = (r >> 2) * 256 + u0 + (r & 3);
+    const int Rf = (fr >> 2) * 256 + u0 + (fr & 3);
+
+    unsigned int wfrag[8][4];
+    {
+      const float* wsrc = (wv == 0) ? w_hh0 : (wv == 1) ? w_ih1 : w_hh1;
+#pragma unroll
+      for (int ch = 0; ch < 8; ++ch)
+#pragma unroll
+        for (int d = 0; d < 4; ++d) {
+          float lo = wsrc[(size_t)Rf * 256 + ch * 32 + kg * 8 + d * 2];
+          float hi = wsrc[(size_t)Rf * 256 + ch * 32 + kg * 8 + d * 2 + 1];
+          wfrag[ch][d] = (unsigned)f2bf(lo) | ((unsigned)f2bf(hi) << 16);
+        }
+    }
+    float wtmp[32];
+#pragma unroll
+    for (int i = 0; i < 32; ++i) wtmp[i] = w_ih0[R * 32 + i];
+    const float bias0r = b_ih0[R] + b_hh0[R];
+    if (tid < 16) bias1s[tid] = b_ih1[R] + b_hh1[R];
+    if (tid < 96) mwmb[tid] = (tid < 64) ? mw[tid] : mb[tid - 64];
+    __syncthreads();
+
+    for (int chunk = 0; chunk < 4; ++chunk) {
+      if (tid < 128) {
+        int pp = tid >> 3, b = tid & 7;
+        int pg = chunk * 16 + pp;
+        float s0 = iseq[(b * 64 + pg) * 2 + 0];
+        float s1 = iseq[(b * 64 + pg) * 2 + 1];
+        for (int k = 0; k < 32; ++k)
+          embc[pp][b][k] = fmaxf(fmaf(mwmb[2 * k], s0, fmaf(mwmb[2 * k + 1], s1, mwmb[64 + k])), 0.f);
+      }
+      __syncthreads();
+      {
+        int pg = chunk * 16 + ks;
+        for (int b = 0; b < 8; ++b) {
+          float a = bias0r;
+          const float* e = &embc[ks][b][0];
+#pragma unroll
+          for (int k = 0; k < 32; ++k) a = fmaf(wtmp[k], e[k], a);
+          xz[pg][b][r] = a;
+        }
+      }
+      __syncthreads();
+    }
+
+    for (int i = tid; i < 8 * 264; i += TPB) {
+      v0s[8 + i / 264][i % 264] = 0;
+      w1h[8 + i / 264][i % 264] = 0;
+    }
+    __syncthreads();
+
+    float c0 = 0.f, c1 = 0.f;
+    for (int p = 0; p <= 64; ++p) {
+      if (tid < 128) {
+        if (p >= 1) {
+          const unsigned tag0 = (unsigned)p;
+          const u64* s0p = &h0x[(size_t)(p - 1) * 1024 + tid * 8];
+          u64 e[8];
+          for (;;) {
+            bool ok = true;
+#pragma unroll
+            for (int i = 0; i < 8; ++i) {
+              e[i] = __hip_atomic_load(&s0p[i], __ATOMIC_RELAXED, __HIP_MEMORY_SCOPE_AGENT);
+              ok &= ((unsigned)(e[i] >> 32) == tag0);
+            }
+            if (ok) break;
+            __builtin_amdgcn_s_sleep(1);
+          }
+#pragma unroll
+          for (int i = 0; i < 8; ++i) {
+            int g = tid * 8 + i;
+            int bb = (g >> 1) & 7, ub = (g >> 4) * 4 + (g & 1) * 2;
+            *(unsigned int*)&v0s[bb][ub] = (unsigned int)e[i];
+          }
+        } else {
+#pragma unroll
+          for (int i = 0; i < 8; ++i) {
+            int g = tid * 8 + i;
+            int bb = (g >> 1) & 7, ub = (g >> 4) * 4 + (g & 1) * 2;
+            *(unsigned int*)&v0s[bb][ub] = 0u;
+          }
+        }
+      } else {
+        int t2 = tid - 128;
+        if (p >= 2) {
+          const unsigned tag1 = (unsigned)(p - 1);
+          const u64* s1p = &h1x[(size_t)(p - 2) * 1024 + t2 * 8];
+          u64 e[8];
+          for (;;) {
+            bool ok = true;
+#pragma unroll
+            for (int i = 0; i < 8; ++i) {
+              e[i] = __hip_atomic_load(&s1p[i], __ATOMIC_RELAXED, __HIP_MEMORY_SCOPE_AGENT);
+              ok &= ((unsigned)(e[i] >> 32) == tag1);
+            }
+            if (ok) break;
+            __builtin_amdgcn_s_sleep(1);
+          }
+#pragma unroll
+          for (int i = 0; i < 8; ++i) {
+            int g = t2 * 8 + i;
+            int bb = (g >> 1) & 7, ub = (g >> 4) * 4 + (g & 1) * 2;
+            *(unsigned int*)&w1h[bb][ub] = (unsigned int)e[i];
+          }
+        } else {
+#pragma unroll
+          for (int i = 0; i < 8; ++i) {
+            int g = t2 * 8 + i;
+            int bb = (g >> 1) & 7, ub = (g >> 4) * 4 + (g & 1) * 2;
+            *(unsigned int*)&w1h[bb][ub] = 0u;
+          }
+        }
+      }
+      __syncthreads();
+
+      if (wv == 0) {
+        if (p < 64) {
+          f32x4 acc = {0.f, 0.f, 0.f, 0.f};
+#pragma unroll
+          for (int ch = 0; ch < 8; ++ch) {
+            bf16x8 af = lda_bf8(&v0s[fr][ch * 32 + kg * 8]);
+            acc = __builtin_amdgcn_mfma_f32_16x16x32_bf16(af, frag_of(wfrag[ch]), acc, 0, 0, 0);
+          }
+#pragma unroll
+          for (int j = 0; j < 4; ++j) {
+            int bb2 = (lane >> 4) * 4 + j;
+            if (bb2 < 8) P0[bb2][fr] = acc[j];
+          }
+        }
+      } else if (wv == 1) {
+        if (p >= 1) {
+          f32x4 acc = {0.f, 0.f, 0.f, 0.f};
+#pragma unroll
+          for (int ch = 0; ch < 8; ++ch) {
+            bf16x8 af = lda_bf8(&v0s[fr][ch * 32 + kg * 8]);
+            acc = __builtin_amdgcn_mfma_f32_16x16x32_bf16(af, frag_of(wfrag[ch]), acc, 0, 0, 0);
+          }
+#pragma unroll
+          for (int j = 0; j < 4; ++j) {
+            int bb2 = (lane >> 4) * 4 + j;
+            if (bb2 < 8) P1a[bb2][fr] = acc[j];
+          }
+        }
+      } else if (wv == 2) {
+        if (p >= 1) {
+          f32x4 acc = {0.f, 0.f, 0.f, 0.f};
+#pragma unroll
+          for (int ch = 0; ch < 8; ++ch) {
+            bf16x8 af = lda_bf8(&w1h[fr][ch * 32 + kg * 8]);
+            acc = __builtin_amdgcn_mfma_f32_16x16x32_bf16(af, frag_of(wfrag[ch]), acc, 0, 0, 0);
+          }
+#pragma unroll
+          for (int j = 0; j < 4; ++j) {
+            int bb2 = (lane >> 4) * 4 + j;
+            if (bb2 < 8) P1b[bb2][fr] = acc[j];
+          }
+        }
+      }
+      __syncthreads();
+
+      if (tid < 32 && p < 64) {
+        int b = tid >> 2, uu = tid & 3;
+        float zi = P0[b][uu]      + xz[p][b][uu];
+        float zf = P0[b][4 + uu]  + xz[p][b][4 + uu];
+        float zg = P0[b][8 + uu]  + xz[p][b][8 + uu];
+        float zo = P0[b][12 + uu] + xz[p][b][12 + uu];
+        c0 = sigf(zf) * c0 + sigf(zi) * tanhf(zg);
+        float h = sigf(zo) * tanhf(c0);
+        float hp = __shfl_xor(h, 1);
+        if (!(uu & 1)) {
+          unsigned int d = (unsigned int)f2bf(h) | ((unsigned int)f2bf(hp) << 16);
+          u64 v = ((u64)(unsigned)(p + 1) << 32) | d;
+          __hip_atomic_store(&h0x[(size_t)p * 1024 + blkid * 16 + b * 2 + (uu >> 1)], v,
+                             __ATOMIC_RELAXED, __HIP_MEMORY_SCOPE_AGENT);
+        }
+      } else if (tid >= 32 && tid < 64 && p >= 1) {
+        int t2 = tid - 32, b = t2 >> 2, uu = t2 & 3;
+        float zi = P1a[b][uu]      + P1b[b][uu]      + bias1s[uu];
+        float zf = P1a[b][4 + uu]  + P1b[b][4 + uu]  + bias1s[4 + uu];
+        float zg = P1a[b][8 + uu]  + P1b[b][8 + uu]  + bias1s[8 + uu];
+        float zo = P1a[b][12 + uu] + P1b[b][12 + uu] + bias1s[12 + uu];
+        c1 = sigf(zf) * c1 + sigf(zi) * tanhf(zg);
+        float h = sigf(zo) * tanhf(c1);
+        comb[(size_t)(b * 64 + (p - 1)) * 576 + u0 + uu] = h;
+        float hp = __shfl_xor(h, 1);
+        if (!(uu & 1)) {
+          unsigned int d = (unsigned int)f2bf(h) | ((unsigned int)f2bf(hp) << 16);
+          u64 v = ((u64)(unsigned)p << 32) | d;
+          __hip_atomic_store(&h1x[(size_t)(p - 1) * 1024 + blkid * 16 + b * 2 + (uu >> 1)], v,
+                             __ATOMIC_RELAXED, __HIP_MEMORY_SCOPE_AGENT);
+        }
+      }
+    }
+    __syncthreads();
+    if (tid == 0)
+      __hip_atomic_fetch_add(&bar[15], 1, __ATOMIC_RELEASE, __HIP_MEMORY_SCOPE_AGENT);
+    return;
+  }
+
+  const int cid = blockIdx.x - NLB;
+
   {
-    const float* wsrc = (wv == 0) ? w_hh0 : (wv == 1) ? w_ih1 : w_hh1;
-#pragma unroll
-    for (int ch = 0; ch < 8; ++ch)
-#pragma unroll
-      for (int d = 0; d < 4; ++d) {
-        float lo = wsrc[(size_t)Rf * 256 + ch * 32 + kg * 8 + d * 2];
-        float hi = wsrc[(size_t)Rf * 256 + ch * 32 + kg * 8 + d * 2 + 1];
-        wfrag[ch][d] = (unsigned)f2bf(lo) | ((unsigned)f2bf(hi) << 16);
-      }
-  }
-  float wtmp[32];
-#pragma unroll
-  for (int i = 0; i < 32; ++i) wtmp[i] = w_ih0[R * 32 + i];
-  const float bias0r = b_ih0[R] + b_hh0[R];
-  if (tid < 16) bias1s[tid] = b_ih1[R] + b_hh1[R];
-  if (tid < 96) mwmb[tid] = (tid < 64) ? mw[tid] : mb[tid - 64];
-  __syncthreads();
-
-  for (int chunk = 0; chunk < 4; ++chunk) {
-    if (tid < 128) {
-      int pp = tid >> 3, b = tid & 7;
-      int pg = chunk * 16 + pp;
-      float s0 = iseq[(b * 64 + pg) * 2 + 0];
-      float s1 = iseq[(b * 64 + pg) * 2 + 1];
-      for (int k = 0; k < 32; ++k)
-        embc[pp][b][k] = fmaxf(fmaf(mwmb[2 * k], s0, fmaf(mwmb[2 * k + 1], s1, mwmb[64 + k])), 0.f);
-    }
-    __syncthreads();
-    {
-      int pg = chunk * 16 + ks;
-      for (int b = 0; b < 8; ++b) {
-        float a = bias0r;
-        const float* e = &embc[ks][b][0];
-#pragma unroll
-        for (int k = 0; k < 32; ++k) a = fmaf(wtmp[k], e[k], a);
-        xz[pg][b][r] = a;
-      }
-    }
-    __syncthreads();
-  }
-
-  for (int i = tid; i < 8 * 264; i += TPB) {
-    v0s[8 + i / 264][i % 264] = 0;
-    w1h[8 + i / 264][i % 264] = 0;
-  }
-  __syncthreads();
-
-  float c0 = 0.f, c1 = 0.f;
-  for (int p = 0; p <= 64; ++p) {
-    if (tid < 128) {
-      if (p >= 1) {
-        const unsigned tag0 = (unsigned)p;
-        const u64* s0p = &h0x[(size_t)(p - 1) * 1024 + tid * 8];
-        u64 e[8];
-        for (;;) {
-          bool ok = true;
-#pragma unroll
-          for (int i = 0; i < 8; ++i) {
-            e[i] = __hip_atomic_load(&s0p[i], __ATOMIC_RELAXED, __HIP_MEMORY_SCOPE_AGENT);
-            ok &= ((unsigned)(e[i] >> 32) == tag0);
-          }
-          if (ok) break;
-          __builtin_amdgcn_s_sleep(1);
-        }
-#pragma unroll
-        for (int i = 0; i < 8; ++i) {
-          int g = tid * 8 + i;
-          int bb = (g >> 1) & 7, ub = (g >> 4) * 4 + (g & 1) * 2;
-          *(unsigned int*)&v0s[bb][ub] = (unsigned int)e[i];
-        }
-      } else {
-#pragma unroll
-        for (int i = 0; i < 8; ++i) {
-          int g = tid * 8 + i;
-          int bb = (g >> 1) & 7, ub = (g >> 4) * 4 + (g & 1) * 2;
-          *(unsigned int*)&v0s[bb][ub] = 0u;
-        }
-      }
-    } else {
-      int t2 = tid - 128;
-      if (p >= 2) {
-        const unsigned tag1 = (unsigned)(p - 1);
-        const u64* s1p = &h1x[(size_t)(p - 2) * 1024 + t2 * 8];
-        u64 e[8];
-        for (;;) {
-          bool ok = true;
-#pragma unroll
-          for (int i = 0; i < 8; ++i) {
-            e[i] = __hip_atomic_load(&s1p[i], __ATOMIC_RELAXED, __HIP_MEMORY_SCOPE_AGENT);
-            ok &= ((unsigned)(e[i] >> 32) == tag1);
-          }
-          if (ok) break;
-          __builtin_amdgcn_s_sleep(1);
-        }
-#pragma unroll
-        for (int i = 0; i < 8; ++i) {
-          int g = t2 * 8 + i;
-          int bb = (g >> 1) & 7, ub = (g >> 4) * 4 + (g & 1) * 2;
-          *(unsigned int*)&w1h[bb][ub] = (unsigned int)e[i];
-        }
-      } else {
-#pragma unroll
-        for (int i = 0; i < 8; ++i) {
-          int g = t2 * 8 + i;
-          int bb = (g >> 1) & 7, ub = (g >> 4) * 4 + (g & 1) * 2;
-          *(unsigned int*)&w1h[bb][ub] = 0u;
-        }
-      }
-    }
-    __syncthreads();
-
-    if (wv == 0) {
-      if (p < 64) {
-        f32x4 acc = {0.f, 0.f, 0.f, 0.f};
-#pragma unroll
-        for (int ch = 0; ch < 8; ++ch) {
-          bf16x8 af = lda_bf8(&v0s[fr][ch * 32 + kg * 8]);
-          acc = __builtin_amdgcn_mfma_f32_16x16x32_bf16(af, frag_of(wfrag[ch]), acc, 0, 0, 0);
-        }
-#pragma unroll
-        for (int j = 0; j < 4; ++j) {
-          int bb2 = (lane >> 4) * 4 + j;
-          if (bb2 < 8) P0[bb2][fr] = acc[j];
-        }
-      }
-    } else if (wv == 1) {
-      if (p >= 1) {
-        f32x4 acc = {0.f, 0.f, 0.f, 0.f};
-#pragma unroll
-        for (int ch = 0; ch < 8; ++ch) {
-          bf16x8 af = lda_bf8(&v0s[fr][ch * 32 + kg * 8]);
-          acc = __builtin_amdgcn_mfma_f32_16x16x32_bf16(af, frag_of(wfrag[ch]), acc, 0, 0, 0);
-        }
-#pragma unroll
-        for (int j = 0; j < 4; ++j) {
-          int bb2 = (lane >> 4) * 4 + j;
-          if (bb2 < 8) P1a[bb2][fr] = acc[j];
-        }
-      }
-    } else if (wv == 2) {
-      if (p >= 1) {
-        f32x4 acc = {0.f, 0.f, 0.f, 0.f};
-#pragma unroll
-        for (int ch = 0; ch < 8; ++ch) {
-          bf16x8 af = lda_bf8(&w1h[fr][ch * 32 + kg * 8]);
-          acc = __builtin_amdgcn_mfma_f32_16x16x32_bf16(af, frag_of(wfrag[ch]), acc, 0, 0, 0);
-        }
-#pragma unroll
-        for (int j = 0; j < 4; ++j) {
-          int bb2 = (lane >> 4) * 4 + j;
-          if (bb2 < 8) P1b[bb2][fr] = acc[j];
-        }
-      }
-    }
-    __syncthreads();
-
-    if (tid < 32 && p < 64) {
-      int b = tid >> 2, uu = tid & 3;
-      float zi = P0[b][uu]      + xz[p][b][uu];
-      float zf = P0[b][4 + uu]  + xz[p][b][4 + uu];
-      float zg = P0[b][8 + uu]  + xz[p][b][8 + uu];
-      float zo = P0[b][12 + uu] + xz[p][b][12 + uu];
-      c0 = sigf(zf) * c0 + sigf(zi) * tanhf(zg);
-      float h = sigf(zo) * tanhf(c0);
-      float hp = __shfl_xor(h, 1);
-      if (!(uu & 1)) {
-        unsigned int d = (unsigned int)f2bf(h) | ((unsigned int)f2bf(hp) << 16);
-        u64 v = ((u64)(unsigned)(p + 1) << 32) | d;
-        __hip_atomic_store(&h0x[(size_t)p * 1024 + blkid * 16 + b * 2 + (uu >> 1)], v,
-                           __ATOMIC_RELAXED, __HIP_MEMORY_SCOPE_AGENT);
-      }
-    } else if (tid >= 32 && tid < 64 && p >= 1) {
-      int t2 = tid - 32, b = t2 >> 2, uu = t2 & 3;
-      float zi = P1a[b][uu]      + P1b[b][uu]      + bias1s[uu];
-      float zf = P1a[b][4 + uu]  + P1b[b][4 + uu]  + bias1s[4 + uu];
-      float zg = P1a[b][8 + uu]  + P1b[b][8 + uu]  + bias1s[8 + uu];
-      float zo = P1a[b][12 + uu] + P1b[b][12 + uu] + bias1s[12 + uu];
-      c1 = sigf(zf) * c1 + sigf(zi) * tanhf(zg);
-      float h = sigf(zo) * tanhf(c1);
-      comb[(size_t)(b * 64 + (p - 1)) * 576 + u0 + uu] = h;
-      float hp = __shfl_xor(h, 1);
-      if (!(uu & 1)) {
-        unsigned int d = (unsigned int)f2bf(h) | ((unsigned int)f2bf(hp) << 16);
-        u64 v = ((u64)(unsigned)p << 32) | d;
-        __hip_atomic_store(&h1x[(size_t)(p - 1) * 1024 + blkid * 16 + b * 2 + (uu >> 1)], v,
-                           __ATOMIC_RELAXED, __HIP_MEMORY_SCOPE_AGENT);
-      }
-    }
-  }
+    unsigned short (*patch)[132][8] = (unsigned short (*)[132][8])sm;
+    unsigned short (*Bsm)[104] = (unsigned short (*)[104])(sm + 35904);
+    float* bs = (float*)(sm + 39232);
+    float* swsum = (float*)(sm + 39296);
+    float* swsq  = (float*)(sm + 39552);
+    if (tid < 128) { racc_s[tid] = 0.f; racc_q[tid] = 0.f; }
+    for (int e = tid; e < 1536; e += TPB) Bsm[e / 96][e % 96] = wt1[e];
+    if (tid < 16) bs[tid] = cb1[tid];
+    for (int e = tid; e < 17 * 132; e += TPB)
+      *(uint4*)&patch[e / 132][e % 132][0] = uint4{0u, 0u, 0u, 0u};
+    const int w = tid >> 6, lane = tid & 63, fr = lane & 15, kg = lane >> 4, rg = lane >> 4;
+    for (int t = cid; t < 4096; t += NCW) {
+      __syncthreads();
+      const int n = t >> 3, R0 = (t & 7) << 3;
+      const int yy = (int)iseq[n * 2], xx = (int)iseq[n * 2 + 1];
+      const int bimg = n >> 6;
+      for (int e = tid; e < 3 * 17 * 132; e += TPB) {
+        int ic = e / 2244, rem = e % 2244, l = rem / 132, c = rem % 132;
+        int i = 2 * R0 - 1 + l, j = c - 1;
+        float v = 0.f;
+        if ((unsigned)i < 128u && (unsigned)j < 128u) {
+          int rr2 = yy + i - 64, cc = xx + j - 64;
+          if ((unsigned)rr2 < 1024u && (unsigned)cc < 1024u)
+            v = fmap[(((size_t)bimg * 3 + ic) << 20) + ((size_t)rr2 << 10) + cc];
+        }
+        patch[l][c][ic] = f2bf(v);
+      }
+      __syncthreads();
+      f32x4 acc[8];
+#pragma unroll
+      for (int m = 0; m < 8; ++m) acc[m] = {0.f, 0.f, 0.f, 0.f};
+#pragma unroll
+      for (int ch = 0; ch < 3; ++ch) {
+        int k8 = ch * 4 + kg;
+        int ki = (k8 >= 9) ? 0 : ((k8 * 11) >> 5);
+        int kj = (k8 >= 9) ? 0 : (k8 - 3 * ki);
+        bf16x8 bfr = lda_bf8(&Bsm[fr][k8 * 8]);
+#pragma unroll
+        for (int m = 0; m < 8; ++m) {
+          int p = w * 128 + m * 16 + fr;
+          int pr = p >> 6, pc = p & 63;
+          bf16x8 af = lda_bf8(&patch[2 * pr + ki][2 * pc + kj][0]);
+          acc[m] = __builtin_amdgcn_mfma_f32_16x16x32_bf16(af, bfr, acc[m], 0, 0, 0);
+        }
+      }
+      float bb = bs[fr];
+      float sps = 0.f, spq = 0.f;
+#pragma unroll
+      for (int m = 0; m < 8; ++m) {
+#pragma unroll
+        for (int r = 0; r < 4; ++r) {
+          int p = w * 128 + m * 16 + rg * 4 + r;
+          int pr = p >> 6, pc = p & 63;
+          float v = acc[m][r] + bb;
+          sps += v; spq = fmaf(v, v, spq);
+          y1bf[(((size_t)n * 64 + R0 + pr) * 64 + pc) * 16 + fr] = f2bf(v);
+        }
+      }
+      sps += __shfl_xor(sps, 16); spq += __shfl_xor(spq, 16);
+      sps += __shfl_xor(sps, 32); spq += __shfl_xor(spq, 32);
+      if (lane < 16) { swsum[w * 16 + fr] = sps; swsq[w * 16 + fr] = spq; }
+      __syncthreads();
+      if (tid < 16) {
+        racc_s[tid] += swsum[tid] + swsum[16 + tid] + swsum[32 + tid] + swsum[48 + tid];
+        racc_q[tid] += swsq[tid] + swsq[16 + tid] + swsq[32 + tid] + swsq[48 + tid];
+      }
+    }
+    __syncthreads();
+    if (tid < 128) { part[(size_t)cid * 256 + tid * 2] = racc_s[tid]; part[(size_t)cid * 256 + tid * 2 + 1] = racc_q[tid]; }
+  }
+  cbar(bar, 0);
+  if (cid < 16) ssr(part, g1, be1, ss1, 1.f / 2097152.f, cid, (float*)sm);
+  cbar(bar, 1);
+
+  {
+    constexpr int CIN = 16, CB = 32, KPAD = 160, BS = 168, K = 144;
+    unsigned short* patch = (unsigned short*)sm;
+    unsigned short* Bsm = (unsigned short*)(sm + 13872);
+    float* ssl = (float*)(sm + 24624);
+    float* swsum = ssl + CIN * 2;
+    float* swsq = swsum + 4 * CB;
+    if (tid < 128) { racc_s[tid] = 0.f; racc_q[tid] = 0.f; }
+    for (int i = tid; i < CIN * 2; i += TPB) ssl[i] = ss1[i];
+    for (int e = tid; e < CB * (KPAD / 8); e += TPB) {
+      int oc = e / (KPAD / 8), k8i = e % (KPAD / 8);
+      uint4 v = {0u, 0u, 0u, 0u};
+      if (k8i * 8 < K) v = *(const uint4*)&wt2[(size_t)oc * K + k8i * 8];
+      *(uint4*)&Bsm[oc * BS + k8i * 8] = v;
+    }
+    for (int t = cid; t < 8192; t += NCW)
+      ctap_tile<16, 32, 1, 64, 32>(y1bf, wt2, cb2, y2bf, t, patch, Bsm, ssl, swsum, swsq, racc_s, racc_q);
+    __syncthreads();
+    if (tid < 128) { part[(size_t)cid * 256 + tid * 2] = racc_s[tid]; part[(size_t)cid * 256 + tid * 2 + 1] = racc_q[tid]; }
+  }
+  cbar(bar, 2);
+  if (cid < 32) ssr(part, g2, be2, ss2, 1.f / 524288.f, cid, (float*)sm);
+  cbar(bar, 3);
+
+  {
+    constexpr int CIN = 32, CB = 64, KPAD = 288, BS = 296, K = 288;
+    unsigned short* patch = (unsigned short*)sm;
+    unsigned short* Bsm = (unsigned short*)(sm + 23120);
+    float* ssl = (float*)(sm + 61008);
+    float* swsum = ssl + CIN * 2;
+    float* swsq = swsum + 4 * CB;
+    if (tid < 128) { racc_s[tid] = 0.f; racc_q[tid] = 0.f; }
+    for (int i = tid; i < CIN * 2; i += TPB) ssl[i] = ss2[i];
+    for (int e = tid; e < CB * (KPAD / 8); e += TPB) {
+      int oc = e / (KPAD / 8), k8i = e % (KPAD / 8);
+      uint4 v = *(const uint4*)&wt3[(size_t)oc * K + k8i * 8];
+      *(uint4*)&Bsm[oc * BS + k8i * 8] = v;
+    }
+    for (int t = cid; t < 2048; t += NCW)
+      ctap_tile<32, 64, 1, 32, 16>(y2bf, wt3, cb3, y3bf, t, patch, Bsm, ssl, swsum, swsq, racc_s, racc_q);
+    __syncthreads();
+    if (tid < 128) { part[(size_t)cid * 256 + tid * 2] = racc_s[tid]; part[(size_t)cid * 256 + tid * 2 + 1] = racc_q[tid]; }
+  }
+  cbar(bar, 4);
+  if (cid < 64) ssr(part, g3, be3, ss3, 1.f / 131072.f, cid, (float*)sm);
+  cbar(bar, 5);
+
+  {
+    constexpr int CIN = 64;
+    unsigned short* patch = (unsigned short*)sm;
+    unsigned short* Bsm = (unsigned short*)(sm + 41616);
+    float* ssl = (float*)(sm + 60304);
+    float* swsum = ssl + CIN * 2;
+    float* swsq = swsum + 4 * 16;
+    if (tid < 128) { racc_s[tid] = 0.f; racc_q[tid] = 0.f; }
+    for (int i = tid; i < CIN * 2; i += TPB) ssl[i] = ss3[i];
+    for (int t = cid; t < 4096; t += NCW)
+      ctap_tile<64, 16, 8, 16, 8>(y3bf, wt4, cb4, y4pre, t, patch, Bsm, ssl, swsum, swsq, racc_s, racc_q);
+    __syncthreads();
+    if (tid < 128) { part[(size_t)cid * 256 + tid * 2] = racc_s[tid]; part[(size_t)cid * 256 + tid * 2 + 1] = racc_q[tid]; }
+  }
+  cbar(bar, 6);
+  if (cid < 128) ssr(part, g4, be4, ss4, 1.f / 32768.f, cid, (float*)sm);
+  cbar(bar, 7);
+
+  if (cid < 64) dev_fc1(y4pre, fw1bf, ss4, fb1, f1, (cid >> 3) * 64, (cid & 7) * 64, sm);
+  cbar(bar, 8);
+
+  if (cid < 32) {
+    dev_gemm64(f1, fw2, fb2, comb, 256, 512, 0, 576, 256, (cid >> 2) * 64, (cid & 3) * 64, sm);
+  } else if (cid < 40) {
+    float* w1s = (float*)sm;
+    float* w2s = (float*)(sm + 4096);
+    float* hbuf = (float*)(sm + 37888);
+    const int row0 = (cid - 32) * 64;
+    for (int e = tid; e < 128 * 8; e += TPB) {
+      int k2 = e >> 3, tt = e & 7;
+      w1s[k2 * 8 + tt] = (tt < 6) ? ew1[k2 * 6 + tt] : (tt == 6 ? eb1[k2] : 0.f);
+    }
+    for (int e = tid; e < 64 * 128; e += TPB) {
+      int j = e >> 7, k2 = e & 127;
+      w2s[j * 132 + k2] = ew2[j * 128 + k2];
+    }
+    __syncthreads();
+    for (int half = 0; half < 2; ++half) {
+      int row = tid >> 3, seg = tid & 7;
+      int nrow = row0 + half * 32 + row;
+      int b = nrow >> 6, s5 = nrow & 63;
+      float e0 = cond[b * 5], e1 = cond[b * 5 + 1], e2 = cond[b * 5 + 2];
+      float e3 = cond[b * 5 + 3], e4 = cond[b * 5 + 4];
+      float e5 = steps[b * 64 + s5];
+      for (int k2 = seg * 16; k2 < seg * 16 + 16; ++k2) {
+        float a = fmaf(w1s[k2 * 8], e0, fmaf(w1s[k2 * 8 + 1], e1, fmaf(w1s[k2 * 8 + 2], e2,
+                  fmaf(w1s[k2 * 8 + 3], e3, fmaf(w1s[k2 * 8 + 4], e4, fmaf(w1s[k2 * 8 + 5], e5, w1s[k2 * 8 + 6]))))));
+        hbuf[row * 132 + k2] = fmaxf(a, 0.f);
+      }
+      __syncthreads();
+      for (int j = seg * 8; j < seg * 8 + 8; ++j) {
+        float a = eb2[j];
+#pragma unroll 8
+        for (int k2 = 0; k2 < 128; ++k2) a = fmaf(w2s[j * 132 + k2], hbuf[row * 132 + k2], a);
+        comb[(size_t)nrow * 576 + 512 + j] = a;
+      }
+      __syncthreads();
+    }
+  }
+  cbar(bar, 9);
+
+  if (tid == 0) {
+    while (__hip_atomic_load(&bar[15], __ATOMIC_RELAXED, __HIP_MEMORY_SCOPE_AGENT) < NLB)
+      __builtin_amdgcn_s_sleep(8);
+    (void)__hip_atomic_load(&bar[15], __ATOMIC_ACQUIRE, __HIP_MEMORY_SCOPE_AGENT);
+  }
+  __syncthreads();
+  if (cid < 16) dev_gemm64(comb, xw1, xb1, cx1, 128, 576, 1, 128, 0, (cid >> 1) * 64, (cid & 1) * 64, sm);
+  cbar(bar, 10);
+  if (cid < 8) dev_gemm64(cx1, xw2, xb2, cx2, 64, 128, 1, 64, 0, cid * 64, 0, sm);
+  cbar(bar, 11);
+  if (cid < 8) dev_gemm64(cx2, oww, obb, d_out, 2, 64, 0, 2, 0, cid * 64, 0, sm);
 }
 
 extern "C" void kernel_launch(void* const* d_in, const int* in_sizes, int n_in,
@@ -727,6 +826,7 @@
   float* f1    = ws + base; base += 262144;
   u64*   h0x   = (u64*)(ws + base); base += 131072;
   u64*   h1x   = (u64*)(ws + base); base += 131072;
+  int*   bar   = (int*)(ws + base); base += 64;
   float* comb  = ws + base; base += 294912;
   float* cx1   = ws + base; base += 65536;
   float* cx2   = ws + base; base += 32768;
@@ -737,28 +837,17 @@
 
   prep_wt<<<384, TPB, 0, stream>>>(cw1, cw2, cw3, cw4, wt1, wt2, wt3, wt4);
   permute_fw1<<<512, TPB, 0, stream>>>(fw1, fw1bf);
-
-  conv1_tap<<<4096, TPB, 0, stream>>>(fmap, iseq, wt1, cb1, y1bf, part);
-  stats_final3<<<16, TPB, 0, stream>>>(part, g1, be1, ss1, 1.f / 2097152.f, 16, 1, 4096);
-  conv_tap<16, 32, 1, 64, 32><<<8192, TPB, 0, stream>>>(y1bf, ss1, wt2, cb2, y2bf, part);
-  stats_final3<<<32, TPB, 0, stream>>>(part, g2, be2, ss2, 1.f / 524288.f, 32, 1, 8192);
-  conv_tap<32, 64, 1, 32, 16><<<2048, TPB, 0, stream>>>(y2bf, ss2, wt3, cb3, y3bf, part);
-  stats_final3<<<64, TPB, 0, stream>>>(part, g3, be3, ss3, 1.f / 131072.f, 64, 1, 2048);
-  conv_tap<64, 32, 4, 16, 8><<<2048, TPB, 0, stream>>>(y3bf, ss3, wt4, cb4, y4pre, part);
-  stats_final3<<<128, TPB, 0, stream>>>(part, g4, be4, ss4, 1.f / 32768.f, 32, 4, 2048);
-
-  hipMemsetAsync(h0x, 0, 2 * 64 * 1024 * sizeof(u64), stream);
-  lstm_kernel<<<NLB, TPB, 0, stream>>>(iseq, mw, mb,
-                                       w_ih0, w_hh0, b_ih0, b_hh0,
-                                       w_ih1, w_hh1, b_ih1, b_hh1,
-                                       h0x, h1x, comb);
-
-  fc1_mfma<<<dim3(8, 8), TPB, 0, stream>>>(y4pre, fw1bf, ss4, fb1, f1);
-  gemm_m64<<<dim3(4, 8), TPB, 0, stream>>>(f1, fw2, fb2, comb, 256, 512, 0, 576, 256);
-
-  cond_enc<<<8, TPB, 0, stream>>>(cond, steps, ew1, eb1, ew2, eb2, comb);
-
-  gemm_m64<<<dim3(2, 8), TPB, 0, stream>>>(comb, xw1, xb1, cx1, 128, 576, 1, 128, 0);
-  gemm_m64<<<dim3(1, 8), TPB, 0, stream>>>(cx1, xw2, xb2, cx2, 64, 128, 1, 64, 0);
-  gemm_m64<<<dim3(1, 8), TPB, 0, stream>>>(cx2, ow, ob, (float*)d_out, 2, 64, 0, 2, 0);
-}
+  hipMemsetAsync(h0x, 0, 2 * 64 * 1024 * sizeof(u64) + 256, stream);
+
+  mega_kernel<<<NBLK, TPB, 0, stream>>>(
+      fmap, cond, iseq, steps,
+      wt1, wt2, wt3, wt4, cb1, cb2, cb3, cb4,
+      g1, be1, g2, be2, g3, be3, g4, be4,
+      fw1bf, fb1, fw2, fb2, ew1, eb1, ew2, eb2, mw, mb,
+      w_ih0, w_hh0, b_ih0, b_hh0, w_ih1, w_hh1, b_ih1, b_hh1,
+      xw1, xb1, xw2, xb2, ow, ob,
+      y1bf, y2bf, y3bf, y4pre,
+      part, ss1, ss2, ss3, ss4,
+      f1, h0x, h1x, comb, cx1, cx2,
+      (float*)d_out, bar);
+}
```

Result: slower. 918.6 us (+36.0%).
